# Kernel tuning notes

Measured on AMD Instinct MI355X. Metric: run time of the kernel, lower is better.

## Reference

```python
import jax, jax.numpy as jnp
import numpy as np
from jax import lax

B, S, H, E, P, K, R = 64, 512, 768, 32, 16, 9, 6
HEADS, C1, C2 = 4, 128, 64
FEAT = 4 * C2 + 1  # e1, e2, e1*e2, context (64 each) + log-distance


def _ln(x, g, b):
    m = x.mean(-1, keepdims=True)
    v = ((x - m) ** 2).mean(-1, keepdims=True)
    return (x - m) * lax.rsqrt(v + 1e-5) * g + b


def _gat(x, adj, W, a_s, a_d, bias, heads, cout, concat):
    # Dense GATConv over a small fully-masked entity graph. adj[b,i,j]=edge j->i (incl. self-loops).
    h = jnp.einsum('bef,fhc->behc', x, W.reshape(x.shape[-1], heads, cout))
    s = jnp.einsum('behc,hc->bhe', h, a_s)  # source-node attention term
    d = jnp.einsum('behc,hc->bhe', h, a_d)  # target-node attention term
    logits = jax.nn.leaky_relu(d[:, :, :, None] + s[:, :, None, :], 0.2)  # [b,h,i,j]
    logits = jnp.where(adj[:, None, :, :], logits, -1e9)
    att = jax.nn.softmax(logits, axis=-1)
    out = jnp.einsum('bhij,bjhc->bihc', att, h)
    out = out.reshape(out.shape[0], out.shape[1], heads * cout) if concat else out.mean(2)
    return out + bias


def _crf_nll(em, tags, mask, start, end, trans):
    # torchcrf: loss = -mean log-likelihood. em [B,S,K]; tags [B,S]; mask [B,S] bool.
    emt = jnp.transpose(em, (1, 0, 2))
    tgt = tags.T
    mkt = mask.T.astype(em.dtype)
    num0 = start[tgt[0]] + jnp.take_along_axis(emt[0], tgt[0][:, None], 1)[:, 0]

    def nstep(c, inp):
        ptag, sc = c
        e, t, m = inp
        step = trans[ptag, t] + jnp.take_along_axis(e, t[:, None], 1)[:, 0]
        return (jnp.where(m > 0, t, ptag), sc + step * m), None

    (ltag, num), _ = lax.scan(nstep, (tgt[0], num0), (emt[1:], tgt[1:], mkt[1:]))
    num = num + end[ltag]
    a0 = start[None, :] + emt[0]

    def dstep(a, inp):
        e, m = inp
        nxt = jax.scipy.special.logsumexp(a[:, :, None] + trans[None] + e[:, None, :], axis=1)
        return jnp.where(m[:, None] > 0, nxt, a), None

    aT, _ = lax.scan(dstep, a0, (emt[1:], mkt[1:]))
    Z = jax.scipy.special.logsumexp(aT + end[None], axis=1)
    return jnp.mean(Z - num)


def setup_inputs() -> dict:
    key = jax.random.key(0)
    ks = jax.random.split(key, 24)
    n = lambda i, shape, s=0.05: jax.random.normal(ks[i], shape, jnp.float32) * s
    return {
        'sequence_output': jax.random.normal(ks[0], (B, S, H), jnp.float32),
        'attention_mask': jnp.ones((B, S), jnp.int32),
        'ner_labels': jax.random.randint(ks[1], (B, S), 0, K),
        'entity_start': jax.random.randint(ks[2], (B, E), 0, S - 8),
        'entity_len': jax.random.randint(ks[3], (B, E), 0, 8),
        'pair_e1': jax.random.randint(ks[4], (B, P), 0, E),
        'pair_e2': jax.random.randint(ks[5], (B, P), 0, E),
        'pair_labels': jax.random.randint(ks[6], (B, P), 0, 2),
        'adj_mask': jnp.ones((B, E, E), bool),
        'w_ner1': n(7, (H, 256)), 'b_ner1': jnp.zeros((256,), jnp.float32),
        'w_ner2': n(8, (256, K)), 'b_ner2': jnp.zeros((K,), jnp.float32),
        'crf_start': n(9, (K,), 0.1), 'crf_end': n(10, (K,), 0.1), 'crf_trans': n(11, (K, K), 0.1),
        'w_gat1': n(12, (H, HEADS * C1)), 'a_src1': n(13, (HEADS, C1)), 'a_dst1': n(14, (HEADS, C1)),
        'b_gat1': jnp.zeros((HEADS * C1,), jnp.float32),
        'w_gat2': n(15, (HEADS * C1, C2)), 'a_src2': n(16, (1, C2)), 'a_dst2': n(17, (1, C2)),
        'b_gat2': jnp.zeros((C2,), jnp.float32),
        'w_fe': n(18, (FEAT, 512)), 'b_fe': jnp.zeros((512,), jnp.float32),
        'g_fe': jnp.ones((512,), jnp.float32), 'be_fe': jnp.zeros((512,), jnp.float32),
        'w_rc1': n(19, (R, 512, 256)), 'b_rc1': jnp.zeros((R, 256), jnp.float32),
        'g_rc': jnp.ones((R, 256), jnp.float32), 'be_rc': jnp.zeros((R, 256), jnp.float32),
        'w_rc2': n(20, (R, 256, 1)), 'b_rc2': jnp.zeros((R,), jnp.float32),
    }


def reference(sequence_output, attention_mask, ner_labels, entity_start, entity_len,
              pair_e1, pair_e2, pair_labels, adj_mask,
              w_ner1, b_ner1, w_ner2, b_ner2, crf_start, crf_end, crf_trans,
              w_gat1, a_src1, a_dst1, b_gat1, w_gat2, a_src2, a_dst2, b_gat2,
              w_fe, b_fe, g_fe, be_fe, w_rc1, b_rc1, g_rc, be_rc, w_rc2, b_rc2):
    # NER head (dropout off / eval)
    ner_logits = jnp.maximum(sequence_output @ w_ner1 + b_ner1, 0.0) @ w_ner2 + b_ner2
    ner_loss = _crf_nll(ner_logits, ner_labels, attention_mask.astype(bool),
                        crf_start, crf_end, crf_trans)
    # entity span mean-pool via inclusive cumsum trick
    cs = jnp.concatenate([jnp.zeros((B, 1, H), sequence_output.dtype),
                          jnp.cumsum(sequence_output, axis=1)], axis=1)
    e_end = jnp.clip(entity_start + entity_len, 0, S - 1)
    seg = (jnp.take_along_axis(cs, (e_end + 1)[:, :, None], 1)
           - jnp.take_along_axis(cs, entity_start[:, :, None], 1))
    ent = seg / (e_end - entity_start + 1).astype(sequence_output.dtype)[:, :, None]  # [B,E,H]
    x = _gat(ent, adj_mask, w_gat1, a_src1, a_dst1, b_gat1, HEADS, C1, True)
    x = jnp.maximum(x, 0.0)
    x = _gat(x, adj_mask, w_gat2, a_src2, a_dst2, b_gat2, 1, C2, False)  # [B,E,64]
    x1 = jnp.take_along_axis(x, pair_e1[:, :, None], 1)
    x2 = jnp.take_along_axis(x, pair_e2[:, :, None], 1)
    ctx = jnp.broadcast_to(x.mean(1, keepdims=True), (B, P, C2))
    dist = jnp.log(jnp.abs(pair_e1 - pair_e2).astype(x.dtype) + 1.0)[:, :, None]
    pf = jnp.concatenate([x1, x2, x1 * x2, ctx, dist], axis=-1)  # [B,P,257]
    fe = jax.nn.leaky_relu(_ln(pf @ w_fe + b_fe, g_fe, be_fe), 0.01)
    h1 = jnp.einsum('bpf,rfo->rbpo', fe, w_rc1) + b_rc1[:, None, None, :]
    h1 = jax.nn.leaky_relu(_ln(h1, g_rc[:, None, None, :], be_rc[:, None, None, :]), 0.01)
    z = jnp.einsum('rbpo,ro->rbp', h1, w_rc2[:, :, 0]) + b_rc2[:, None, None]
    y = pair_labels.astype(z.dtype)[None]
    # BCEWithLogitsLoss(pos_weight=2.0), mean per relation type, summed over types
    bce = -(2.0 * y * jax.nn.log_sigmoid(z) + (1.0 - y) * jax.nn.log_sigmoid(-z))
    rel_loss = bce.mean(axis=(1, 2)).sum()
    total = ner_loss + rel_loss
    return ner_logits, z, total
```

## Files before the change

kernel.cpp:

```cpp
#include <hip/hip_runtime.h>
#include <math.h>


#define NB 64
#define NS 512
#define NH 768
#define NE 32
#define NP 16
#define NK 9
#define NR 6
#define NHEADS 4
#define NC1 128
#define NC2 64
#define SEGS 16
#define SEGLEN 32

#define ZOFF 294912
#define TOTOFF 301056

#define WS_ENT   0u
#define WS_WG1T  1572864u
#define WS_X1    2621440u
#define WS_X2    3801088u
#define WS_PF    3956736u
#define WS_FE    4222976u
#define WS_CRF   4747264u
#define WS_REL   4747328u
#define WS_W1T   4747392u
#define WS_WRT   0u
#define WS_WFET  393216u
#define WS_SEG   475136u

typedef __attribute__((ext_vector_type(8))) short bf16x8;
typedef __attribute__((ext_vector_type(4))) float f32x4;

__device__ __forceinline__ unsigned short f2bf(float x) {
  union { float f; unsigned u; } v; v.f = x;
  unsigned r = v.u + 0x7FFFu + ((v.u >> 16) & 1u);
  return (unsigned short)(r >> 16);
}

__device__ __forceinline__ float logsigf(float x) {
  if (x >= 0.f) return -log1pf(__expf(-x));
  return x - log1pf(__expf(x));
}

__global__ __launch_bounds__(256) void k_wt(const float* __restrict__ w1,
    const float* __restrict__ wg1, unsigned short* __restrict__ w1t,
    unsigned short* __restrict__ wg1t) {
  __shared__ unsigned short tr[32 * 776];
  const int t = threadIdx.x;
  const float* src;
  unsigned short* dst;
  int c0, ncol;
  if (blockIdx.x < 8) { src = w1; dst = w1t; ncol = 256; c0 = blockIdx.x * 32; }
  else { src = wg1; dst = wg1t; ncol = 512; c0 = (blockIdx.x - 8) * 32; }
#pragma unroll
  for (int p = 0; p < 24; p++) {
    const int k = p * 32 + (t >> 3), c4 = t & 7;
    const float4 f = *reinterpret_cast<const float4*>(&src[(size_t)k * ncol + c0 + c4 * 4]);
    tr[(c4 * 4 + 0) * 776 + k] = f2bf(f.x);
    tr[(c4 * 4 + 1) * 776 + k] = f2bf(f.y);
    tr[(c4 * 4 + 2) * 776 + k] = f2bf(f.z);
    tr[(c4 * 4 + 3) * 776 + k] = f2bf(f.w);
  }
  __syncthreads();
  const int c = t >> 3, q = t & 7;
#pragma unroll
  for (int i = 0; i < 12; i++) {
    *reinterpret_cast<uint4*>(&dst[(size_t)(c0 + c) * NH + q * 96 + i * 8]) =
        *reinterpret_cast<const uint4*>(&tr[c * 776 + q * 96 + i * 8]);
  }
}

__global__ __launch_bounds__(256) void k_wconv(const float* __restrict__ wrc,
    const float* __restrict__ wfe, unsigned short* __restrict__ wrt,
    unsigned short* __restrict__ wfet) {
  __shared__ unsigned short tr[256 * 72];
  const int t = threadIdx.x;
  if (blockIdx.x < 48) {
    const int r = blockIdx.x >> 3, kt = blockIdx.x & 7;
    const int k0 = kt * 64;
#pragma unroll
    for (int i = 0; i < 16; i++) {
      const int slot = t + 256 * i;
      const int row = slot >> 6, c4 = slot & 63;
      const float4 f = *reinterpret_cast<const float4*>(
          &wrc[((size_t)(r * 512) + k0 + row) * 256 + c4 * 4]);
      tr[(c4 * 4 + 0) * 72 + row] = f2bf(f.x);
      tr[(c4 * 4 + 1) * 72 + row] = f2bf(f.y);
      tr[(c4 * 4 + 2) * 72 + row] = f2bf(f.z);
      tr[(c4 * 4 + 3) * 72 + row] = f2bf(f.w);
    }
    __syncthreads();
#pragma unroll
    for (int i = 0; i < 8; i++) {
      const int slot = t + 256 * i;
      const int col = slot >> 3, q = slot & 7;
      *reinterpret_cast<uint4*>(&wrt[((size_t)(r * 256 + col)) * 512 + k0 + q * 8]) =
          *reinterpret_cast<const uint4*>(&tr[col * 72 + q * 8]);
    }
  } else {
    const int bid = blockIdx.x - 48;
    const int kt = bid % 5, cb = bid / 5;
    const int k0 = kt * 64, c0 = cb * 256;
#pragma unroll
    for (int i = 0; i < 16; i++) {
      const int slot = t + 256 * i;
      const int row = slot >> 6, c4 = slot & 63;
      const int k = k0 + row;
      float4 f = {0.f, 0.f, 0.f, 0.f};
      if (k < 257)
        f = *reinterpret_cast<const float4*>(&wfe[(size_t)k * 512 + c0 + c4 * 4]);
      tr[(c4 * 4 + 0) * 72 + row] = f2bf(f.x);
      tr[(c4 * 4 + 1) * 72 + row] = f2bf(f.y);
      tr[(c4 * 4 + 2) * 72 + row] = f2bf(f.z);
      tr[(c4 * 4 + 3) * 72 + row] = f2bf(f.w);
    }
    __syncthreads();
#pragma unroll
    for (int i = 0; i < 8; i++) {
      const int slot = t + 256 * i;
      const int col = slot >> 3, q = slot & 7;
      *reinterpret_cast<uint4*>(&wfet[((size_t)(c0 + col)) * 320 + k0 + q * 8]) =
          *reinterpret_cast<const uint4*>(&tr[col * 72 + q * 8]);
    }
  }
}

__global__ __launch_bounds__(256) void k_ner(const float* __restrict__ seq,
    const unsigned short* __restrict__ w1t, const float* __restrict__ b1,
    const float* __restrict__ w2, const float* __restrict__ b2,
    float* __restrict__ out) {
  __shared__ unsigned short AsS[64 * 40];
  __shared__ unsigned short BsS[256 * 40];
  __shared__ float zs[64 * 4 * 12];
  const int t = threadIdx.x;
  const int tok0 = blockIdx.x * 64;
  const int w = t >> 6, lane = t & 63, quad = lane >> 4, l15 = lane & 15;

  f32x4 acc[4][4];
#pragma unroll
  for (int r = 0; r < 4; r++)
#pragma unroll
    for (int c = 0; c < 4; c++) acc[r][c] = (f32x4){0.f, 0.f, 0.f, 0.f};

  const int tokA = t >> 2, koffA = (t & 3) * 8;
  const float* aptr = seq + (size_t)(tok0 + tokA) * NH + koffA;

  for (int kt = 0; kt < NH; kt += 32) {
    __syncthreads();
    {
      const float4 f0 = *reinterpret_cast<const float4*>(aptr + kt);
      const float4 f1 = *reinterpret_cast<const float4*>(aptr + kt + 4);
      bf16x8 av;
      av[0] = (short)f2bf(f0.x); av[1] = (short)f2bf(f0.y);
      av[2] = (short)f2bf(f0.z); av[3] = (short)f2bf(f0.w);
      av[4] = (short)f2bf(f1.x); av[5] = (short)f2bf(f1.y);
      av[6] = (short)f2bf(f1.z); av[7] = (short)f2bf(f1.w);
      *reinterpret_cast<bf16x8*>(&AsS[tokA * 40 + koffA]) = av;
    }
#pragma unroll
    for (int i = 0; i < 4; i++) {
      const int q = t + 256 * i;
      const int col = q >> 2, koff = (q & 3) * 8;
      *reinterpret_cast<uint4*>(&BsS[col * 40 + koff]) =
          *reinterpret_cast<const uint4*>(&w1t[(size_t)col * NH + kt + koff]);
    }
    __syncthreads();
    bf16x8 a[4], b[4];
#pragma unroll
    for (int r = 0; r < 4; r++)
      a[r] = *reinterpret_cast<const bf16x8*>(&AsS[(r * 16 + l15) * 40 + quad * 8]);
#pragma unroll
    for (int c = 0; c < 4; c++)
      b[c] = *reinterpret_cast<const bf16x8*>(&BsS[(w * 64 + c * 16 + l15) * 40 + quad * 8]);
#pragma unroll
    for (int r = 0; r < 4; r++)
#pragma unroll
      for (int c = 0; c < 4; c++)
        acc[r][c] = __builtin_amdgcn_mfma_f32_16x16x32_bf16(a[r], b[c], acc[r][c], 0, 0, 0);
  }

  float b1v[4], w2v[4][NK];
#pragma unroll
  for (int c = 0; c < 4; c++) {
    const int col = w * 64 + c * 16 + l15;
    b1v[c] = b1[col];
#pragma unroll
    for (int cc = 0; cc < NK; cc++) w2v[c][cc] = w2[col * NK + cc];
  }
#pragma unroll
  for (int r = 0; r < 4; r++) {
#pragma unroll
    for (int reg = 0; reg < 4; reg++) {
      float p[NK];
#pragma unroll
      for (int cc = 0; cc < NK; cc++) p[cc] = 0.f;
#pragma unroll
      for (int c = 0; c < 4; c++) {
        const float h = fmaxf(acc[r][c][reg] + b1v[c], 0.f);
#pragma unroll
        for (int cc = 0; cc < NK; cc++) p[cc] = fmaf(h, w2v[c][cc], p[cc]);
      }
#pragma unroll
      for (int o = 1; o < 16; o <<= 1)
#pragma unroll
        for (int cc = 0; cc < NK; cc++) p[cc] += __shfl_xor(p[cc], o);
      if (l15 == 0) {
        const int tokr = r * 16 + quad * 4 + reg;
#pragma unroll
        for (int cc = 0; cc < NK; cc++) zs[(tokr * 4 + w) * 12 + cc] = p[cc];
      }
    }
  }
  __syncthreads();
  if (t < 64) {
#pragma unroll
    for (int cc = 0; cc < NK; cc++) {
      const float z = zs[(t * 4 + 0) * 12 + cc] + zs[(t * 4 + 1) * 12 + cc] +
                      zs[(t * 4 + 2) * 12 + cc] + zs[(t * 4 + 3) * 12 + cc] + b2[cc];
      out[(size_t)(tok0 + t) * NK + cc] = z;
    }
  }
}

__global__ __launch_bounds__(128) void k_crf_seg(const float* __restrict__ em,
    const int* __restrict__ mask, const float* __restrict__ trans,
    float* __restrict__ segm) {
  __shared__ float bufA[16 * 81];
  __shared__ float bufB[8 * 81];
  __shared__ float ems[SEGLEN * 9];
  __shared__ int mks[SEGLEN];
  __shared__ float trs[81];
  const int blk = blockIdx.x;
  const int b = blk >> 4, seg = blk & 15;
  const int t = threadIdx.x;
  const int s0 = 1 + seg * SEGLEN;
  const float* emb = em + (size_t)b * NS * NK;
  const int* mk = mask + b * NS;
  if (t < 81) trs[t] = trans[t];
  for (int i = t; i < SEGLEN * 9; i += 128) {
    const int g = s0 * 9 + i;
    ems[i] = (g < NS * 9) ? emb[g] : 0.f;
  }
  if (t < SEGLEN) {
    const int s = s0 + t;
    mks[t] = (s < NS) ? mk[s] : 0;
  }
  __syncthreads();
  for (int idx = t; idx < 16 * 81; idx += 128) {
    const int p = idx / 81, e = idx % 81, i = e / 9, j = e % 9;
    const int la = 2 * p, lb = la + 1;
    const bool ma = mks[la] > 0, mb = mks[lb] > 0;
    float r;
    if (ma && mb) {
      float v[9], mx = -1e30f;
#pragma unroll
      for (int m = 0; m < 9; m++) {
        v[m] = trs[i * 9 + m] + ems[la * 9 + m] + trs[m * 9 + j];
        mx = fmaxf(mx, v[m]);
      }
      float sum = 0.f;
#pragma unroll
      for (int m = 0; m < 9; m++) sum += __expf(v[m] - mx);
      r = mx + __logf(sum) + ems[lb * 9 + j];
    } else if (ma) {
      r = trs[e] + ems[la * 9 + j];
    } else if (mb) {
      r = trs[e] + ems[lb * 9 + j];
    } else {
      r = (i == j) ? 0.f : -1e30f;
    }
    bufA[p * 81 + e] = r;
  }
  float* src = bufA;
  float* dst = bufB;
  for (int n = 16; n > 1; n >>= 1) {
    __syncthreads();
    const int half = n >> 1;
    for (int idx = t; idx < half * 81; idx += 128) {
      const int q = idx / 81, e = idx % 81, i = e / 9, j = e % 9;
      const float* A = src + (size_t)(2 * q) * 81;
      const float* Bm = src + (size_t)(2 * q + 1) * 81;
      float v[9], mx = -1e30f;
#pragma unroll
      for (int m = 0; m < 9; m++) {
        v[m] = A[i * 9 + m] + Bm[m * 9 + j];
        mx = fmaxf(mx, v[m]);
      }
      float sum = 0.f;
#pragma unroll
      for (int m = 0; m < 9; m++) sum += __expf(v[m] - mx);
      dst[q * 81 + e] = mx + __logf(sum);
    }
    float* tmp = src; src = dst; dst = tmp;
  }
  __syncthreads();
  if (t < 81) segm[((size_t)b * SEGS + seg) * 81 + t] = src[t];
}

__global__ __launch_bounds__(64) void k_crf_fin(const float* __restrict__ em,
    const int* __restrict__ tags, const int* __restrict__ mask,
    const float* __restrict__ startv, const float* __restrict__ endv,
    const float* __restrict__ trans, const float* __restrict__ segm,
    float* __restrict__ lossb) {
  __shared__ float sm[SEGS * 81];
  __shared__ float av[16];
  __shared__ float red[2];
  const int b = blockIdx.x, t = threadIdx.x;
  const float* emb = em + (size_t)b * NS * NK;
  const int* mk = mask + b * NS;
  const int* tg = tags + b * NS;
  for (int i = t; i < SEGS * 81; i += 64) sm[i] = segm[(size_t)b * SEGS * 81 + i];
  {
    float num = 0.f;
    int lastS = 0;
#pragma unroll
    for (int o = 0; o < 8; o++) {
      const int s = t * 8 + o;
      if (s >= 1 && mk[s] > 0) {
        const int cur = tg[s], prv = tg[s - 1];
        num += trans[prv * NK + cur] + emb[s * NK + cur];
        lastS = s;
      }
    }
#pragma unroll
    for (int o = 32; o > 0; o >>= 1) {
      num += __shfl_xor(num, o);
      lastS = max(lastS, __shfl_xor(lastS, o));
    }
    if (t == 0) {
      const int t0 = tg[0];
      red[0] = startv[t0] + emb[t0] + num + endv[tg[lastS]];
    }
  }
  __syncthreads();
  if (t < 9) av[t] = startv[t] + emb[t];
  __syncthreads();
  for (int h = 0; h < SEGS; h++) {
    float nv = 0.f;
    if (t < 9) {
      float v[9], mx = -1e30f;
#pragma unroll
      for (int i2 = 0; i2 < 9; i2++) {
        v[i2] = av[i2] + sm[h * 81 + i2 * 9 + t];
        mx = fmaxf(mx, v[i2]);
      }
      float sum = 0.f;
#pragma unroll
      for (int i2 = 0; i2 < 9; i2++) sum += __expf(v[i2] - mx);
      nv = mx + __logf(sum);
    }
    __syncthreads();
    if (t < 9) av[t] = nv;
    __syncthreads();
  }
  if (t == 0) {
    float mx = -1e30f;
#pragma unroll
    for (int j = 0; j < 9; j++) mx = fmaxf(mx, av[j] + endv[j]);
    float sum = 0.f;
#pragma unroll
    for (int j = 0; j < 9; j++) sum += __expf(av[j] + endv[j] - mx);
    lossb[b] = (mx + __logf(sum)) - red[0];
  }
}

__global__ __launch_bounds__(256) void k_ent(const float* __restrict__ seq,
    const int* __restrict__ est, const int* __restrict__ elen,
    unsigned short* __restrict__ entb) {
  const int be = blockIdx.x;
  const int b = be >> 5, e = be & 31;
  const int st = est[b * NE + e];
  int en = st + elen[b * NE + e];
  en = min(max(en, 0), NS - 1);
  const float inv = 1.f / (float)(en - st + 1);
  for (int c = threadIdx.x; c < NH; c += 256) {
    float s = 0.f;
    for (int r = st; r <= en; r++) s += seq[((size_t)b * NS + r) * NH + c];
    entb[((size_t)b * NE + e) * NH + c] = f2bf(s * inv);
  }
}

__global__ __launch_bounds__(256) void k_g1f(const unsigned short* __restrict__ entb,
    const unsigned short* __restrict__ wg1t, const float* __restrict__ as,
    const float* __restrict__ ad, const unsigned char* __restrict__ adj,
    const float* __restrict__ bias, float* __restrict__ x1) {
  __shared__ unsigned short As[32 * 40];
  __shared__ unsigned short Bs[128 * 40];
  __shared__ float Hs[32 * 132];
  __shared__ float Att[32 * 32];
  __shared__ float Sv[32], Dv[32];
  const int b = blockIdx.x >> 2, hd = blockIdx.x & 3;
  const int t = threadIdx.x;
  const int w = t >> 6, lane = t & 63, quad = lane >> 4, l15 = lane & 15;

  f32x4 acc[2][2];
#pragma unroll
  for (int r = 0; r < 2; r++)
#pragma unroll
    for (int c = 0; c < 2; c++) acc[r][c] = (f32x4){0.f, 0.f, 0.f, 0.f};

  const int rowA = t >> 2, koffA = (t & 3) * 8;
  const unsigned short* aptr = entb + ((size_t)(b * NE) + rowA) * NH + koffA;

  for (int kt = 0; kt < NH; kt += 32) {
    __syncthreads();
    if (t < 128) {
      *reinterpret_cast<uint4*>(&As[rowA * 40 + koffA]) =
          *reinterpret_cast<const uint4*>(aptr + kt);
    }
#pragma unroll
    for (int i = 0; i < 2; i++) {
      const int q = t + 256 * i;
      const int col = q >> 2, koff = (q & 3) * 8;
      *reinterpret_cast<uint4*>(&Bs[col * 40 + koff]) =
          *reinterpret_cast<const uint4*>(&wg1t[(size_t)(hd * 128 + col) * NH + kt + koff]);
    }
    __syncthreads();
    bf16x8 a[2], bb[2];
#pragma unroll
    for (int r = 0; r < 2; r++)
      a[r] = *reinterpret_cast<const bf16x8*>(&As[(r * 16 + l15) * 40 + quad * 8]);
#pragma unroll
    for (int c = 0; c < 2; c++)
      bb[c] = *reinterpret_cast<const bf16x8*>(&Bs[(w * 32 + c * 16 + l15) * 40 + quad * 8]);
#pragma unroll
    for (int r = 0; r < 2; r++)
#pragma unroll
      for (int c = 0; c < 2; c++)
        acc[r][c] = __builtin_amdgcn_mfma_f32_16x16x32_bf16(a[r], bb[c], acc[r][c], 0, 0, 0);
  }
#pragma unroll
  for (int r = 0; r < 2; r++)
#pragma unroll
    for (int c = 0; c < 2; c++)
#pragma unroll
      for (int reg = 0; reg < 4; reg++)
        Hs[(r * 16 + quad * 4 + reg) * 132 + w * 32 + c * 16 + l15] = acc[r][c][reg];
  __syncthreads();
  {
    const int e = t >> 3, cg = t & 7;
    float sv = 0.f, dv = 0.f;
#pragma unroll
    for (int c = 0; c < 16; c++) {
      const float h = Hs[e * 132 + cg * 16 + c];
      sv += h * as[hd * NC1 + cg * 16 + c];
      dv += h * ad[hd * NC1 + cg * 16 + c];
    }
#pragma unroll
    for (int o = 1; o < 8; o <<= 1) { sv += __shfl_xor(sv, o); dv += __shfl_xor(dv, o); }
    if (cg == 0) { Sv[e] = sv; Dv[e] = dv; }
  }
  __syncthreads();
  if (t < 32) {
    const int i = t;
    const float di = Dv[i];
    float lg[32];
    float m = -1e30f;
#pragma unroll
    for (int j = 0; j < 32; j++) {
      float v = di + Sv[j];
      v = v >= 0.f ? v : 0.2f * v;
      if (!adj[((size_t)b * NE + i) * NE + j]) v = -1e9f;
      lg[j] = v; m = fmaxf(m, v);
    }
    float sum = 0.f;
#pragma unroll
    for (int j = 0; j < 32; j++) { lg[j] = __expf(lg[j] - m); sum += lg[j]; }
    const float inv = 1.f / sum;
#pragma unroll
    for (int j = 0; j < 32; j++) Att[j * 32 + i] = lg[j] * inv;
  }
  __syncthreads();
  {
    const int tc = t & 31, tr = t >> 5;
#pragma unroll
    for (int i = 0; i < 4; i++) {
      const int row = tr * 4 + i;
      float o0 = bias[hd * NC1 + tc * 4 + 0];
      float o1 = bias[hd * NC1 + tc * 4 + 1];
      float o2 = bias[hd * NC1 + tc * 4 + 2];
      float o3 = bias[hd * NC1 + tc * 4 + 3];
#pragma unroll
      for (int j = 0; j < 32; j++) {
        const float a = Att[j * 32 + row];
        o0 = fmaf(a, Hs[j * 132 + tc * 4 + 0], o0);
        o1 = fmaf(a, Hs[j * 132 + tc * 4 + 1], o1);
        o2 = fmaf(a, Hs[j * 132 + tc * 4 + 2], o2);
        o3 = fmaf(a, Hs[j * 132 + tc * 4 + 3], o3);
      }
      float4 v;
      v.x = fmaxf(o0, 0.f); v.y = fmaxf(o1, 0.f);
      v.z = fmaxf(o2, 0.f); v.w = fmaxf(o3, 0.f);
      *reinterpret_cast<float4*>(&x1[((size_t)b * NE + row) * 512 + hd * 128 + tc * 4]) = v;
    }
  }
}

__global__ __launch_bounds__(256) void k_g2f(const float* __restrict__ x1,
    const float* __restrict__ w, const float* __restrict__ as,
    const float* __restrict__ ad, const unsigned char* __restrict__ adj,
    const float* __restrict__ bias, float* __restrict__ x2) {
  __shared__ float As[32 * 36];
  __shared__ float Bs[32 * 64];
  __shared__ float H2[32 * 68];
  __shared__ float Att[32 * 32];
  __shared__ float Sv[32], Dv[32];
  const int b = blockIdx.x;
  const int t = threadIdx.x;
  const int tc = t & 15, tr = t >> 4;
  float acc[2][4];
#pragma unroll
  for (int i = 0; i < 2; i++)
#pragma unroll
    for (int j = 0; j < 4; j++) acc[i][j] = 0.f;
  for (int kt = 0; kt < 512; kt += 32) {
    __syncthreads();
    {
      const int e = t >> 3, k4 = t & 7;
      *reinterpret_cast<float4*>(&As[e * 36 + k4 * 4]) =
          *reinterpret_cast<const float4*>(&x1[((size_t)b * NE + e) * 512 + kt + k4 * 4]);
    }
#pragma unroll
    for (int i = 0; i < 2; i++) {
      const int slot = t + 256 * i;
      const int row = slot >> 4, cg = slot & 15;
      *reinterpret_cast<float4*>(&Bs[row * 64 + cg * 4]) =
          *reinterpret_cast<const float4*>(&w[(size_t)(kt + row) * NC2 + cg * 4]);
    }
    __syncthreads();
#pragma unroll
    for (int kg = 0; kg < 8; kg++) {
      float4 a[2];
#pragma unroll
      for (int i = 0; i < 2; i++)
        a[i] = *reinterpret_cast<const float4*>(&As[(tr * 2 + i) * 36 + kg * 4]);
#pragma unroll
      for (int k2 = 0; k2 < 4; k2++) {
        const float4 bv = *reinterpret_cast<const float4*>(&Bs[(kg * 4 + k2) * 64 + tc * 4]);
#pragma unroll
        for (int i = 0; i < 2; i++) {
          const float av = reinterpret_cast<const float*>(&a[i])[k2];
          acc[i][0] = fmaf(av, bv.x, acc[i][0]);
          acc[i][1] = fmaf(av, bv.y, acc[i][1]);
          acc[i][2] = fmaf(av, bv.z, acc[i][2]);
          acc[i][3] = fmaf(av, bv.w, acc[i][3]);
        }
      }
    }
  }
  const float4 a4s = *reinterpret_cast<const float4*>(&as[tc * 4]);
  const float4 a4d = *reinterpret_cast<const float4*>(&ad[tc * 4]);
#pragma unroll
  for (int i = 0; i < 2; i++) {
    const int e = tr * 2 + i;
    float4 v;
    v.x = acc[i][0]; v.y = acc[i][1]; v.z = acc[i][2]; v.w = acc[i][3];
    *reinterpret_cast<float4*>(&H2[e * 68 + tc * 4]) = v;
    float sv = v.x * a4s.x + v.y * a4s.y + v.z * a4s.z + v.w * a4s.w;
    float dv = v.x * a4d.x + v.y * a4d.y + v.z * a4d.z + v.w * a4d.w;
#pragma unroll
    for (int o = 8; o > 0; o >>= 1) { sv += __shfl_xor(sv, o); dv += __shfl_xor(dv, o); }
    if (tc == 0) { Sv[e] = sv; Dv[e] = dv; }
  }
  __syncthreads();
  if (t < 32) {
    const int i = t;
    const float di = Dv[i];
    float lg[32];
    float m = -1e30f;
#pragma unroll
    for (int j = 0; j < 32; j++) {
      float v = di + Sv[j];
      v = v >= 0.f ? v : 0.2f * v;
      if (!adj[((size_t)b * NE + i) * NE + j]) v = -1e9f;
      lg[j] = v; m = fmaxf(m, v);
    }
    float sum = 0.f;
#pragma unroll
    for (int j = 0; j < 32; j++) { lg[j] = __expf(lg[j] - m); sum += lg[j]; }
    const float inv = 1.f / sum;
#pragma unroll
    for (int j = 0; j < 32; j++) Att[j * 32 + i] = lg[j] * inv;
  }
  __syncthreads();
#pragma unroll
  for (int i = 0; i < 2; i++) {
    const int row = tr * 2 + i;
    float o0 = bias[tc * 4 + 0];
    float o1 = bias[tc * 4 + 1];
    float o2 = bias[tc * 4 + 2];
    float o3 = bias[tc * 4 + 3];
#pragma unroll
    for (int j = 0; j < 32; j++) {
      const float a = Att[j * 32 + row];
      o0 = fmaf(a, H2[j * 68 + tc * 4 + 0], o0);
      o1 = fmaf(a, H2[j * 68 + tc * 4 + 1], o1);
      o2 = fmaf(a, H2[j * 68 + tc * 4 + 2], o2);
      o3 = fmaf(a, H2[j * 68 + tc * 4 + 3], o3);
    }
    float4 v;
    v.x = o0; v.y = o1; v.z = o2; v.w = o3;
    *reinterpret_cast<float4*>(&x2[((size_t)b * NE + row) * NC2 + tc * 4]) = v;
  }
}

__global__ __launch_bounds__(64) void k_pf(const float* __restrict__ x2,
    const int* __restrict__ pe1, const int* __restrict__ pe2,
    float* __restrict__ pf) {
  const int bp = blockIdx.x;
  const int b = bp >> 4, p = bp & 15;
  const int t = threadIdx.x;
  const int e1 = pe1[b * NP + p], e2 = pe2[b * NP + p];
  const float v1 = x2[((size_t)b * NE + e1) * NC2 + t];
  const float v2 = x2[((size_t)b * NE + e2) * NC2 + t];
  float cs = 0.f;
  for (int e = 0; e < NE; e++) cs += x2[((size_t)b * NE + e) * NC2 + t];
  float* row = pf + (size_t)bp * 260;
  row[t] = v1;
  row[64 + t] = v2;
  row[128 + t] = v1 * v2;
  row[192 + t] = cs * (1.f / NE);
  if (t == 0) row[256] = logf(fabsf((float)(e1 - e2)) + 1.f);
  if (t < 3) row[257 + t] = 0.f;
}

__global__ __launch_bounds__(256) void k_fe(const float* __restrict__ pf,
    const unsigned short* __restrict__ wt, const float* __restrict__ bfe,
    const float* __restrict__ g, const float* __restrict__ be,
    unsigned short* __restrict__ feb) {
  __shared__ unsigned short Af[16 * 320];
  __shared__ float Cs[16 * 520];
  const int b = blockIdx.x, t = threadIdx.x;
  const int w = t >> 6, lane = t & 63, quad = lane >> 4, l15 = lane & 15;
  for (int i = t; i < 16 * 320; i += 256) {
    const int p = i / 320, k = i - p * 320;
    Af[i] = (k < 260) ? f2bf(pf[(size_t)(b * NP + p) * 260 + k]) : (unsigned short)0;
  }
  __syncthreads();
  f32x4 acc[8];
#pragma unroll
  for (int c = 0; c < 8; c++) acc[c] = (f32x4){0.f, 0.f, 0.f, 0.f};
#pragma unroll
  for (int kt = 0; kt < 10; kt++) {
    const bf16x8 a = *reinterpret_cast<const bf16x8*>(&Af[l15 * 320 + kt * 32 + quad * 8]);
#pragma unroll
    for (int c = 0; c < 8; c++) {
      const int col = w * 128 + c * 16 + l15;
      const bf16x8 bv = *reinterpret_cast<const bf16x8*>(&wt[(size_t)col * 320 + kt * 32 + quad * 8]);
      acc[c] = __builtin_amdgcn_mfma_f32_16x16x32_bf16(a, bv, acc[c], 0, 0, 0);
    }
  }
#pragma unroll
  for (int c = 0; c < 8; c++)
#pragma unroll
    for (int reg = 0; reg < 4; reg++)
      Cs[(quad * 4 + reg) * 520 + w * 128 + c * 16 + l15] = acc[c][reg];
  __syncthreads();
  float bfev[8], gv[8], bev[8];
#pragma unroll
  for (int ch = 0; ch < 8; ch++) {
    const int col = ch * 64 + lane;
    bfev[ch] = bfe[col]; gv[ch] = g[col]; bev[ch] = be[col];
  }
#pragma unroll
  for (int pp = 0; pp < 4; pp++) {
    const int p = w * 4 + pp;
    float v[8], s = 0.f, sq = 0.f;
#pragma unroll
    for (int ch = 0; ch < 8; ch++) {
      v[ch] = Cs[p * 520 + ch * 64 + lane] + bfev[ch];
      s += v[ch]; sq += v[ch] * v[ch];
    }
#pragma unroll
    for (int o = 32; o > 0; o >>= 1) { s += __shfl_xor(s, o); sq += __shfl_xor(sq, o); }
    const float mean = s * (1.f / 512.f);
    const float var = sq * (1.f / 512.f) - mean * mean;
    const float rr = rsqrtf(var + 1e-5f);
#pragma unroll
    for (int ch = 0; ch < 8; ch++) {
      float n = (v[ch] - mean) * rr * gv[ch] + bev[ch];
      n = n >= 0.f ? n : 0.01f * n;
      feb[(size_t)(b * NP + p) * 512 + ch * 64 + lane] = f2bf(n);
    }
  }
}

__global__ __launch_bounds__(256) void k_rc(const unsigned short* __restrict__ feb,
    const unsigned short* __restrict__ wrt, const float* __restrict__ b1,
    const float* __restrict__ g, const float* __restrict__ be,
    const float* __restrict__ w2, const float* __restrict__ b2,
    const int* __restrict__ ylab, float* __restrict__ zout, float* __restrict__ relacc) {
  __shared__ unsigned short Af[16 * 520];
  __shared__ float Cs[16 * 264];
  const int blk = blockIdx.x;
  const int r = blk >> 6, b = blk & 63;
  const int t = threadIdx.x;
  const int w = t >> 6, lane = t & 63, quad = lane >> 4, l15 = lane & 15;
#pragma unroll
  for (int i = 0; i < 4; i++) {
    const int slot = t + 256 * i;
    const int p = slot >> 6, q = slot & 63;
    *reinterpret_cast<uint4*>(&Af[p * 520 + q * 8]) =
        *reinterpret_cast<const uint4*>(&feb[(size_t)(b * NP + p) * 512 + q * 8]);
  }
  __syncthreads();
  f32x4 acc[4];
#pragma unroll
  for (int c = 0; c < 4; c++) acc[c] = (f32x4){0.f, 0.f, 0.f, 0.f};
#pragma unroll
  for (int kt = 0; kt < 16; kt++) {
    const bf16x8 a = *reinterpret_cast<const bf16x8*>(&Af[l15 * 520 + kt * 32 + quad * 8]);
#pragma unroll
    for (int c = 0; c < 4; c++) {
      const int col = w * 64 + c * 16 + l15;
      const bf16x8 bv = *reinterpret_cast<const bf16x8*>(
          &wrt[(size_t)(r * 256 + col) * 512 + kt * 32 + quad * 8]);
      acc[c] = __builtin_amdgcn_mfma_f32_16x16x32_bf16(a, bv, acc[c], 0, 0, 0);
    }
  }
#pragma unroll
  for (int c = 0; c < 4; c++)
#pragma unroll
    for (int reg = 0; reg < 4; reg++)
      Cs[(quad * 4 + reg) * 264 + w * 64 + c * 16 + l15] = acc[c][reg];
  __syncthreads();
  float b1v[4], gv[4], bev[4], w2v[4];
#pragma unroll
  for (int ch = 0; ch < 4; ch++) {
    const int col = r * 256 + ch * 64 + lane;
    b1v[ch] = b1[col]; gv[ch] = g[col]; bev[ch] = be[col]; w2v[ch] = w2[col];
  }
  const float b2v = b2[r];
  float local = 0.f;
#pragma unroll
  for (int pp = 0; pp < 4; pp++) {
    const int p = w * 4 + pp;
    float v[4], s = 0.f, sq = 0.f;
#pragma unroll
    for (int ch = 0; ch < 4; ch++) {
      v[ch] = Cs[p * 264 + ch * 64 + lane] + b1v[ch];
      s += v[ch]; sq += v[ch] * v[ch];
    }
#pragma unroll
    for (int o = 32; o > 0; o >>= 1) { s += __shfl_xor(s, o); sq += __shfl_xor(sq, o); }
    const float mean = s * (1.f / 256.f);
    const float var = sq * (1.f / 256.f) - mean * mean;
    const float rr = rsqrtf(var + 1e-5f);
    float zdot = 0.f;
#pragma unroll
    for (int ch = 0; ch < 4; ch++) {
      float n = (v[ch] - mean) * rr * gv[ch] + bev[ch];
      n = n >= 0.f ? n : 0.01f * n;
      zdot = fmaf(n, w2v[ch], zdot);
    }
#pragma unroll
    for (int o = 32; o > 0; o >>= 1) zdot += __shfl_xor(zdot, o);
    if (lane == 0) {
      const float zp = zdot + b2v;
      zout[(size_t)(r * NB + b) * NP + p] = zp;
      const float y = (float)ylab[b * NP + p];
      local += -(2.f * y * logsigf(zp) + (1.f - y) * logsigf(-zp));
    }
  }
  if (lane == 0) atomicAdd(relacc, local * (1.f / (NB * NP)));
}

__global__ __launch_bounds__(64) void k_fin(const float* __restrict__ lossb,
    const float* __restrict__ rel, float* __restrict__ out) {
  float v = lossb[threadIdx.x];
#pragma unroll
  for (int o = 32; o > 0; o >>= 1) v += __shfl_down(v, o);
  if (threadIdx.x == 0) out[TOTOFF] = v * (1.f / NB) + rel[0];
}

extern "C" void kernel_launch(void* const* d_in, const int* in_sizes, int n_in,
                              void* d_out, int out_size, void* d_ws, size_t ws_size,
                              hipStream_t stream) {
  const float* seq = (const float*)d_in[0];
  const int* amask = (const int*)d_in[1];
  const int* nlab = (const int*)d_in[2];
  const int* est = (const int*)d_in[3];
  const int* elen = (const int*)d_in[4];
  const int* pe1 = (const int*)d_in[5];
  const int* pe2 = (const int*)d_in[6];
  const int* plab = (const int*)d_in[7];
  const unsigned char* adj = (const unsigned char*)d_in[8];
  const float* w_ner1 = (const float*)d_in[9];
  const float* b_ner1 = (const float*)d_in[10];
  const float* w_ner2 = (const float*)d_in[11];
  const float* b_ner2 = (const float*)d_in[12];
  const float* crf_start = (const float*)d_in[13];
  const float* crf_end = (const float*)d_in[14];
  const float* crf_trans = (const float*)d_in[15];
  const float* w_gat1 = (const float*)d_in[16];
  const float* a_src1 = (const float*)d_in[17];
  const float* a_dst1 = (const float*)d_in[18];
  const float* b_gat1 = (const float*)d_in[19];
  const float* w_gat2 = (const float*)d_in[20];
  const float* a_src2 = (const float*)d_in[21];
  const float* a_dst2 = (const float*)d_in[22];
  const float* b_gat2 = (const float*)d_in[23];
  const float* w_fe = (const float*)d_in[24];
  const float* b_fe = (const float*)d_in[25];
  const float* g_fe = (const float*)d_in[26];
  const float* be_fe = (const float*)d_in[27];
  const float* w_rc1 = (const float*)d_in[28];
  const float* b_rc1 = (const float*)d_in[29];
  const float* g_rc = (const float*)d_in[30];
  const float* be_rc = (const float*)d_in[31];
  const float* w_rc2 = (const float*)d_in[32];
  const float* b_rc2 = (const float*)d_in[33];

  float* out = (float*)d_out;
  float* ws = (float*)d_ws;
  float* x1 = ws + WS_X1;
  float* x2 = ws + WS_X2;
  float* pf = ws + WS_PF;
  float* crfb = ws + WS_CRF;
  float* rel = ws + WS_REL;
  unsigned short* entb = (unsigned short*)(ws + WS_ENT);
  unsigned short* wg1t = (unsigned short*)(ws + WS_WG1T);
  unsigned short* w1t = (unsigned short*)(ws + WS_W1T);
  unsigned short* feb = (unsigned short*)(ws + WS_FE);
  unsigned short* wrt = (unsigned short*)(ws + WS_WRT);
  unsigned short* wfet = (unsigned short*)(ws + WS_WFET);
  float* segm = ws + WS_SEG;

  hipMemsetAsync(rel, 0, sizeof(float), stream);

  k_wt<<<24, 256, 0, stream>>>(w_ner1, w_gat1, w1t, wg1t);
  k_ner<<<512, 256, 0, stream>>>(seq, w1t, b_ner1, w_ner2, b_ner2, out);
  k_ent<<<NB * NE, 256, 0, stream>>>(seq, est, elen, entb);
  k_g1f<<<NB * NHEADS, 256, 0, stream>>>(entb, wg1t, a_src1, a_dst1, adj, b_gat1, x1);
  k_wconv<<<58, 256, 0, stream>>>(w_rc1, w_fe, wrt, wfet);
  k_crf_seg<<<NB * SEGS, 128, 0, stream>>>(out, amask, crf_trans, segm);
  k_crf_fin<<<NB, 64, 0, stream>>>(out, nlab, amask, crf_start, crf_end, crf_trans,
                                   segm, crfb);
  k_g2f<<<NB, 256, 0, stream>>>(x1, w_gat2, a_src2, a_dst2, adj, b_gat2, x2);
  k_pf<<<NB * NP, 64, 0, stream>>>(x2, pe1, pe2, pf);
  k_fe<<<NB, 256, 0, stream>>>(pf, wfet, b_fe, g_fe, be_fe, feb);
  k_rc<<<NR * NB, 256, 0, stream>>>(feb, wrt, b_rc1, g_rc, be_rc, w_rc2, b_rc2,
                                    plab, out + ZOFF, rel);
  k_fin<<<1, 64, 0, stream>>>(crfb, rel, out);
}
```

Before: 452.0 us.

## Merge independent stages into combined launches and fuse GAT/pair-feature steps

Collapses the pipeline from eleven launches to seven by packing independent work into shared grids. Weight transposes and entity pooling share one kernel. GAT layer 1 runs beside the NER GEMM, now tiled at 32 tokens per block. Weight conversion runs beside the CRF segment pass, and GAT layer 2 (moved to bf16 MFMA with a pre-transposed weight) runs beside the CRF finalisation. Pair-feature construction is folded into k_fe, and x1 is stored as bf16. The aim is to cut launch overhead, fill the GPU with concurrent independent work and drop intermediate buffers, at the cost of heterogeneous blocks with uneven per-block work and a little extra bf16 rounding.

New measurement: 431.9 us. -4.4%, faster.

```diff
diff --git a/kernel.cpp b/kernel.cpp
--- a/kernel.cpp
+++ b/kernel.cpp
@@ -22,7 +22,7 @@
 #define WS_WG1T  1572864u
 #define WS_X1    2621440u
 #define WS_X2    3801088u
-#define WS_PF    3956736u
+#define WS_WG2T  3956736u
 #define WS_FE    4222976u
 #define WS_CRF   4747264u
 #define WS_REL   4747328u
@@ -45,599 +45,597 @@
   return x - log1pf(__expf(x));
 }
 
-__global__ __launch_bounds__(256) void k_wt(const float* __restrict__ w1,
-    const float* __restrict__ wg1, unsigned short* __restrict__ w1t,
-    unsigned short* __restrict__ wg1t) {
+__global__ __launch_bounds__(256) void k_prep(
+    const float* __restrict__ w1, const float* __restrict__ wg1,
+    const float* __restrict__ wg2, const float* __restrict__ seq,
+    const int* __restrict__ est, const int* __restrict__ elen,
+    unsigned short* __restrict__ w1t, unsigned short* __restrict__ wg1t,
+    unsigned short* __restrict__ wg2t, unsigned short* __restrict__ entb) {
   __shared__ unsigned short tr[32 * 776];
-  const int t = threadIdx.x;
-  const float* src;
-  unsigned short* dst;
-  int c0, ncol;
-  if (blockIdx.x < 8) { src = w1; dst = w1t; ncol = 256; c0 = blockIdx.x * 32; }
-  else { src = wg1; dst = wg1t; ncol = 512; c0 = (blockIdx.x - 8) * 32; }
-#pragma unroll
-  for (int p = 0; p < 24; p++) {
-    const int k = p * 32 + (t >> 3), c4 = t & 7;
-    const float4 f = *reinterpret_cast<const float4*>(&src[(size_t)k * ncol + c0 + c4 * 4]);
-    tr[(c4 * 4 + 0) * 776 + k] = f2bf(f.x);
-    tr[(c4 * 4 + 1) * 776 + k] = f2bf(f.y);
-    tr[(c4 * 4 + 2) * 776 + k] = f2bf(f.z);
-    tr[(c4 * 4 + 3) * 776 + k] = f2bf(f.w);
-  }
-  __syncthreads();
-  const int c = t >> 3, q = t & 7;
-#pragma unroll
-  for (int i = 0; i < 12; i++) {
-    *reinterpret_cast<uint4*>(&dst[(size_t)(c0 + c) * NH + q * 96 + i * 8]) =
-        *reinterpret_cast<const uint4*>(&tr[c * 776 + q * 96 + i * 8]);
-  }
-}
-
-__global__ __launch_bounds__(256) void k_wconv(const float* __restrict__ wrc,
-    const float* __restrict__ wfe, unsigned short* __restrict__ wrt,
-    unsigned short* __restrict__ wfet) {
-  __shared__ unsigned short tr[256 * 72];
-  const int t = threadIdx.x;
-  if (blockIdx.x < 48) {
-    const int r = blockIdx.x >> 3, kt = blockIdx.x & 7;
-    const int k0 = kt * 64;
-#pragma unroll
-    for (int i = 0; i < 16; i++) {
-      const int slot = t + 256 * i;
-      const int row = slot >> 6, c4 = slot & 63;
-      const float4 f = *reinterpret_cast<const float4*>(
-          &wrc[((size_t)(r * 512) + k0 + row) * 256 + c4 * 4]);
-      tr[(c4 * 4 + 0) * 72 + row] = f2bf(f.x);
-      tr[(c4 * 4 + 1) * 72 + row] = f2bf(f.y);
-      tr[(c4 * 4 + 2) * 72 + row] = f2bf(f.z);
-      tr[(c4 * 4 + 3) * 72 + row] = f2bf(f.w);
-    }
-    __syncthreads();
-#pragma unroll
-    for (int i = 0; i < 8; i++) {
-      const int slot = t + 256 * i;
-      const int col = slot >> 3, q = slot & 7;
-      *reinterpret_cast<uint4*>(&wrt[((size_t)(r * 256 + col)) * 512 + k0 + q * 8]) =
-          *reinterpret_cast<const uint4*>(&tr[col * 72 + q * 8]);
+  const int bid = blockIdx.x, t = threadIdx.x;
+  if (bid < 26) {
+    const float* src;
+    unsigned short* dst;
+    int c0, ncol, nkt, kdim;
+    if (bid < 8)       { src = w1;  dst = w1t;  ncol = 256; c0 = bid * 32;        nkt = 24; kdim = 768; }
+    else if (bid < 24) { src = wg1; dst = wg1t; ncol = 512; c0 = (bid - 8) * 32;  nkt = 24; kdim = 768; }
+    else               { src = wg2; dst = wg2t; ncol = 64;  c0 = (bid - 24) * 32; nkt = 16; kdim = 512; }
+    for (int p = 0; p < nkt; p++) {
+      const int k = p * 32 + (t >> 3), c4 = t & 7;
+      const float4 f = *reinterpret_cast<const float4*>(&src[(size_t)k * ncol + c0 + c4 * 4]);
+      tr[(c4 * 4 + 0) * 776 + k] = f2bf(f.x);
+      tr[(c4 * 4 + 1) * 776 + k] = f2bf(f.y);
+      tr[(c4 * 4 + 2) * 776 + k] = f2bf(f.z);
+      tr[(c4 * 4 + 3) * 776 + k] = f2bf(f.w);
+    }
+    __syncthreads();
+    const int c = t >> 3, q = t & 7;
+    const int chunk = kdim >> 3;
+    for (int i = 0; i < (chunk >> 3); i++) {
+      *reinterpret_cast<uint4*>(&dst[(size_t)(c0 + c) * kdim + q * chunk + i * 8]) =
+          *reinterpret_cast<const uint4*>(&tr[c * 776 + q * chunk + i * 8]);
     }
   } else {
-    const int bid = blockIdx.x - 48;
-    const int kt = bid % 5, cb = bid / 5;
-    const int k0 = kt * 64, c0 = cb * 256;
-#pragma unroll
-    for (int i = 0; i < 16; i++) {
-      const int slot = t + 256 * i;
-      const int row = slot >> 6, c4 = slot & 63;
-      const int k = k0 + row;
-      float4 f = {0.f, 0.f, 0.f, 0.f};
-      if (k < 257)
-        f = *reinterpret_cast<const float4*>(&wfe[(size_t)k * 512 + c0 + c4 * 4]);
-      tr[(c4 * 4 + 0) * 72 + row] = f2bf(f.x);
-      tr[(c4 * 4 + 1) * 72 + row] = f2bf(f.y);
-      tr[(c4 * 4 + 2) * 72 + row] = f2bf(f.z);
-      tr[(c4 * 4 + 3) * 72 + row] = f2bf(f.w);
-    }
-    __syncthreads();
-#pragma unroll
-    for (int i = 0; i < 8; i++) {
-      const int slot = t + 256 * i;
-      const int col = slot >> 3, q = slot & 7;
-      *reinterpret_cast<uint4*>(&wfet[((size_t)(c0 + col)) * 320 + k0 + q * 8]) =
-          *reinterpret_cast<const uint4*>(&tr[col * 72 + q * 8]);
-    }
-  }
-}
-
-__global__ __launch_bounds__(256) void k_ner(const float* __restrict__ seq,
-    const unsigned short* __restrict__ w1t, const float* __restrict__ b1,
-    const float* __restrict__ w2, const float* __restrict__ b2,
-    float* __restrict__ out) {
-  __shared__ unsigned short AsS[64 * 40];
-  __shared__ unsigned short BsS[256 * 40];
-  __shared__ float zs[64 * 4 * 12];
-  const int t = threadIdx.x;
-  const int tok0 = blockIdx.x * 64;
+    const int be = bid - 26;
+    const int b = be >> 5, e = be & 31;
+    const int st = est[b * NE + e];
+    int en = st + elen[b * NE + e];
+    en = min(max(en, 0), NS - 1);
+    const float inv = 1.f / (float)(en - st + 1);
+    for (int c = t; c < NH; c += 256) {
+      float s = 0.f;
+      for (int r = st; r <= en; r++) s += seq[((size_t)b * NS + r) * NH + c];
+      entb[((size_t)b * NE + e) * NH + c] = f2bf(s * inv);
+    }
+  }
+}
+
+__global__ __launch_bounds__(256) void k_main(
+    const float* __restrict__ seq, const unsigned short* __restrict__ w1t,
+    const float* __restrict__ b1, const float* __restrict__ w2,
+    const float* __restrict__ b2, float* __restrict__ out,
+    const unsigned short* __restrict__ entb, const unsigned short* __restrict__ wg1t,
+    const float* __restrict__ as1, const float* __restrict__ ad1,
+    const unsigned char* __restrict__ adj, const float* __restrict__ bias1,
+    unsigned short* __restrict__ x1b) {
+  __shared__ __align__(16) char smem[34048];
+  const int bid = blockIdx.x, t = threadIdx.x;
   const int w = t >> 6, lane = t & 63, quad = lane >> 4, l15 = lane & 15;
 
-  f32x4 acc[4][4];
-#pragma unroll
-  for (int r = 0; r < 4; r++)
-#pragma unroll
-    for (int c = 0; c < 4; c++) acc[r][c] = (f32x4){0.f, 0.f, 0.f, 0.f};
-
-  const int tokA = t >> 2, koffA = (t & 3) * 8;
-  const float* aptr = seq + (size_t)(tok0 + tokA) * NH + koffA;
-
-  for (int kt = 0; kt < NH; kt += 32) {
+  if (bid < 256) {
+    unsigned short* As = (unsigned short*)smem;
+    unsigned short* Bs = (unsigned short*)(smem + 2560);
+    float* Hs  = (float*)(smem + 12800);
+    float* Att = (float*)(smem + 29696);
+    float* Sv  = (float*)(smem + 33792);
+    float* Dv  = (float*)(smem + 33920);
+    const int b = bid >> 2, hd = bid & 3;
+
+    f32x4 acc[2][2];
+#pragma unroll
+    for (int r = 0; r < 2; r++)
+#pragma unroll
+      for (int c = 0; c < 2; c++) acc[r][c] = (f32x4){0.f, 0.f, 0.f, 0.f};
+
+    const int rowA = t >> 2, koffA = (t & 3) * 8;
+    const unsigned short* aptr = entb + ((size_t)(b * NE) + rowA) * NH + koffA;
+
+    for (int kt = 0; kt < NH; kt += 32) {
+      __syncthreads();
+      if (t < 128) {
+        *reinterpret_cast<uint4*>(&As[rowA * 40 + koffA]) =
+            *reinterpret_cast<const uint4*>(aptr + kt);
+      }
+#pragma unroll
+      for (int i = 0; i < 2; i++) {
+        const int q = t + 256 * i;
+        const int col = q >> 2, koff = (q & 3) * 8;
+        *reinterpret_cast<uint4*>(&Bs[col * 40 + koff]) =
+            *reinterpret_cast<const uint4*>(&wg1t[(size_t)(hd * 128 + col) * NH + kt + koff]);
+      }
+      __syncthreads();
+      bf16x8 a[2], bb[2];
+#pragma unroll
+      for (int r = 0; r < 2; r++)
+        a[r] = *reinterpret_cast<const bf16x8*>(&As[(r * 16 + l15) * 40 + quad * 8]);
+#pragma unroll
+      for (int c = 0; c < 2; c++)
+        bb[c] = *reinterpret_cast<const bf16x8*>(&Bs[(w * 32 + c * 16 + l15) * 40 + quad * 8]);
+#pragma unroll
+      for (int r = 0; r < 2; r++)
+#pragma unroll
+        for (int c = 0; c < 2; c++)
+          acc[r][c] = __builtin_amdgcn_mfma_f32_16x16x32_bf16(a[r], bb[c], acc[r][c], 0, 0, 0);
+    }
+#pragma unroll
+    for (int r = 0; r < 2; r++)
+#pragma unroll
+      for (int c = 0; c < 2; c++)
+#pragma unroll
+        for (int reg = 0; reg < 4; reg++)
+          Hs[(r * 16 + quad * 4 + reg) * 132 + w * 32 + c * 16 + l15] = acc[r][c][reg];
     __syncthreads();
     {
-      const float4 f0 = *reinterpret_cast<const float4*>(aptr + kt);
-      const float4 f1 = *reinterpret_cast<const float4*>(aptr + kt + 4);
-      bf16x8 av;
-      av[0] = (short)f2bf(f0.x); av[1] = (short)f2bf(f0.y);
-      av[2] = (short)f2bf(f0.z); av[3] = (short)f2bf(f0.w);
-      av[4] = (short)f2bf(f1.x); av[5] = (short)f2bf(f1.y);
-      av[6] = (short)f2bf(f1.z); av[7] = (short)f2bf(f1.w);
-      *reinterpret_cast<bf16x8*>(&AsS[tokA * 40 + koffA]) = av;
-    }
-#pragma unroll
-    for (int i = 0; i < 4; i++) {
-      const int q = t + 256 * i;
-      const int col = q >> 2, koff = (q & 3) * 8;
-      *reinterpret_cast<uint4*>(&BsS[col * 40 + koff]) =
-          *reinterpret_cast<const uint4*>(&w1t[(size_t)col * NH + kt + koff]);
-    }
-    __syncthreads();
-    bf16x8 a[4], b[4];
-#pragma unroll
-    for (int r = 0; r < 4; r++)
-      a[r] = *reinterpret_cast<const bf16x8*>(&AsS[(r * 16 + l15) * 40 + quad * 8]);
-#pragma unroll
-    for (int c = 0; c < 4; c++)
-      b[c] = *reinterpret_cast<const bf16x8*>(&BsS[(w * 64 + c * 16 + l15) * 40 + quad * 8]);
-#pragma unroll
-    for (int r = 0; r < 4; r++)
+      const int e = t >> 3, cg = t & 7;
+      float sv = 0.f, dv = 0.f;
+#pragma unroll
+      for (int c = 0; c < 16; c++) {
+        const float h = Hs[e * 132 + cg * 16 + c];
+        sv += h * as1[hd * NC1 + cg * 16 + c];
+        dv += h * ad1[hd * NC1 + cg * 16 + c];
+      }
+#pragma unroll
+      for (int o = 1; o < 8; o <<= 1) { sv += __shfl_xor(sv, o); dv += __shfl_xor(dv, o); }
+      if (cg == 0) { Sv[e] = sv; Dv[e] = dv; }
+    }
+    __syncthreads();
+    if (t < 32) {
+      const int i = t;
+      const float di = Dv[i];
+      float lg[32];
+      float m = -1e30f;
+#pragma unroll
+      for (int j = 0; j < 32; j++) {
+        float v = di + Sv[j];
+        v = v >= 0.f ? v : 0.2f * v;
+        if (!adj[((size_t)b * NE + i) * NE + j]) v = -1e9f;
+        lg[j] = v; m = fmaxf(m, v);
+      }
+      float sum = 0.f;
+#pragma unroll
+      for (int j = 0; j < 32; j++) { lg[j] = __expf(lg[j] - m); sum += lg[j]; }
+      const float inv = 1.f / sum;
+#pragma unroll
+      for (int j = 0; j < 32; j++) Att[j * 32 + i] = lg[j] * inv;
+    }
+    __syncthreads();
+    {
+      const int tc = t & 31, tr2 = t >> 5;
+#pragma unroll
+      for (int i = 0; i < 4; i++) {
+        const int row = tr2 * 4 + i;
+        float o0 = bias1[hd * NC1 + tc * 4 + 0];
+        float o1 = bias1[hd * NC1 + tc * 4 + 1];
+        float o2 = bias1[hd * NC1 + tc * 4 + 2];
+        float o3 = bias1[hd * NC1 + tc * 4 + 3];
+#pragma unroll
+        for (int j = 0; j < 32; j++) {
+          const float a = Att[j * 32 + row];
+          o0 = fmaf(a, Hs[j * 132 + tc * 4 + 0], o0);
+          o1 = fmaf(a, Hs[j * 132 + tc * 4 + 1], o1);
+          o2 = fmaf(a, Hs[j * 132 + tc * 4 + 2], o2);
+          o3 = fmaf(a, Hs[j * 132 + tc * 4 + 3], o3);
+        }
+        uint2 v;
+        v.x = (unsigned)f2bf(fmaxf(o0, 0.f)) | ((unsigned)f2bf(fmaxf(o1, 0.f)) << 16);
+        v.y = (unsigned)f2bf(fmaxf(o2, 0.f)) | ((unsigned)f2bf(fmaxf(o3, 0.f)) << 16);
+        *reinterpret_cast<uint2*>(&x1b[((size_t)b * NE + row) * 512 + hd * 128 + tc * 4]) = v;
+      }
+    }
+  } else {
+    unsigned short* AsS = (unsigned short*)smem;
+    unsigned short* BsS = (unsigned short*)(smem + 2560);
+    float* zs = (float*)(smem + 23040);
+    const int tok0 = (bid - 256) * 32;
+
+    f32x4 acc[2][4];
+#pragma unroll
+    for (int r = 0; r < 2; r++)
+#pragma unroll
+      for (int c = 0; c < 4; c++) acc[r][c] = (f32x4){0.f, 0.f, 0.f, 0.f};
+
+    const int tokA = t >> 3, koffA = (t & 7) * 4;
+    const float* aptr = seq + (size_t)(tok0 + tokA) * NH + koffA;
+
+    for (int kt = 0; kt < NH; kt += 32) {
+      __syncthreads();
+      {
+        const float4 f0 = *reinterpret_cast<const float4*>(aptr + kt);
+        uint2 v;
+        v.x = (unsigned)f2bf(f0.x) | ((unsigned)f2bf(f0.y) << 16);
+        v.y = (unsigned)f2bf(f0.z) | ((unsigned)f2bf(f0.w) << 16);
+        *reinterpret_cast<uint2*>(&AsS[tokA * 40 + koffA]) = v;
+      }
+#pragma unroll
+      for (int i = 0; i < 4; i++) {
+        const int q = t + 256 * i;
+        const int col = q >> 2, koff = (q & 3) * 8;
+        *reinterpret_cast<uint4*>(&BsS[col * 40 + koff]) =
+            *reinterpret_cast<const uint4*>(&w1t[(size_t)col * NH + kt + koff]);
+      }
+      __syncthreads();
+      bf16x8 a[2], b[4];
+#pragma unroll
+      for (int r = 0; r < 2; r++)
+        a[r] = *reinterpret_cast<const bf16x8*>(&AsS[(r * 16 + l15) * 40 + quad * 8]);
 #pragma unroll
       for (int c = 0; c < 4; c++)
-        acc[r][c] = __builtin_amdgcn_mfma_f32_16x16x32_bf16(a[r], b[c], acc[r][c], 0, 0, 0);
-  }
-
-  float b1v[4], w2v[4][NK];
-#pragma unroll
-  for (int c = 0; c < 4; c++) {
-    const int col = w * 64 + c * 16 + l15;
-    b1v[c] = b1[col];
-#pragma unroll
-    for (int cc = 0; cc < NK; cc++) w2v[c][cc] = w2[col * NK + cc];
-  }
-#pragma unroll
-  for (int r = 0; r < 4; r++) {
-#pragma unroll
-    for (int reg = 0; reg < 4; reg++) {
-      float p[NK];
-#pragma unroll
-      for (int cc = 0; cc < NK; cc++) p[cc] = 0.f;
-#pragma unroll
-      for (int c = 0; c < 4; c++) {
-        const float h = fmaxf(acc[r][c][reg] + b1v[c], 0.f);
-#pragma unroll
-        for (int cc = 0; cc < NK; cc++) p[cc] = fmaf(h, w2v[c][cc], p[cc]);
-      }
-#pragma unroll
-      for (int o = 1; o < 16; o <<= 1)
-#pragma unroll
-        for (int cc = 0; cc < NK; cc++) p[cc] += __shfl_xor(p[cc], o);
-      if (l15 == 0) {
-        const int tokr = r * 16 + quad * 4 + reg;
-#pragma unroll
-        for (int cc = 0; cc < NK; cc++) zs[(tokr * 4 + w) * 12 + cc] = p[cc];
-      }
-    }
-  }
-  __syncthreads();
-  if (t < 64) {
-#pragma unroll
-    for (int cc = 0; cc < NK; cc++) {
-      const float z = zs[(t * 4 + 0) * 12 + cc] + zs[(t * 4 + 1) * 12 + cc] +
-                      zs[(t * 4 + 2) * 12 + cc] + zs[(t * 4 + 3) * 12 + cc] + b2[cc];
-      out[(size_t)(tok0 + t) * NK + cc] = z;
-    }
-  }
-}
-
-__global__ __launch_bounds__(128) void k_crf_seg(const float* __restrict__ em,
-    const int* __restrict__ mask, const float* __restrict__ trans,
-    float* __restrict__ segm) {
-  __shared__ float bufA[16 * 81];
-  __shared__ float bufB[8 * 81];
-  __shared__ float ems[SEGLEN * 9];
-  __shared__ int mks[SEGLEN];
-  __shared__ float trs[81];
-  const int blk = blockIdx.x;
-  const int b = blk >> 4, seg = blk & 15;
-  const int t = threadIdx.x;
-  const int s0 = 1 + seg * SEGLEN;
-  const float* emb = em + (size_t)b * NS * NK;
-  const int* mk = mask + b * NS;
-  if (t < 81) trs[t] = trans[t];
-  for (int i = t; i < SEGLEN * 9; i += 128) {
-    const int g = s0 * 9 + i;
-    ems[i] = (g < NS * 9) ? emb[g] : 0.f;
-  }
-  if (t < SEGLEN) {
-    const int s = s0 + t;
-    mks[t] = (s < NS) ? mk[s] : 0;
-  }
-  __syncthreads();
-  for (int idx = t; idx < 16 * 81; idx += 128) {
-    const int p = idx / 81, e = idx % 81, i = e / 9, j = e % 9;
-    const int la = 2 * p, lb = la + 1;
-    const bool ma = mks[la] > 0, mb = mks[lb] > 0;
-    float r;
-    if (ma && mb) {
-      float v[9], mx = -1e30f;
-#pragma unroll
-      for (int m = 0; m < 9; m++) {
-        v[m] = trs[i * 9 + m] + ems[la * 9 + m] + trs[m * 9 + j];
-        mx = fmaxf(mx, v[m]);
+        b[c] = *reinterpret_cast<const bf16x8*>(&BsS[(w * 64 + c * 16 + l15) * 40 + quad * 8]);
+#pragma unroll
+      for (int r = 0; r < 2; r++)
+#pragma unroll
+        for (int c = 0; c < 4; c++)
+          acc[r][c] = __builtin_amdgcn_mfma_f32_16x16x32_bf16(a[r], b[c], acc[r][c], 0, 0, 0);
+    }
+
+    float b1v[4], w2v[4][NK];
+#pragma unroll
+    for (int c = 0; c < 4; c++) {
+      const int col = w * 64 + c * 16 + l15;
+      b1v[c] = b1[col];
+#pragma unroll
+      for (int cc = 0; cc < NK; cc++) w2v[c][cc] = w2[col * NK + cc];
+    }
+#pragma unroll
+    for (int r = 0; r < 2; r++) {
+#pragma unroll
+      for (int reg = 0; reg < 4; reg++) {
+        float p[NK];
+#pragma unroll
+        for (int cc = 0; cc < NK; cc++) p[cc] = 0.f;
+#pragma unroll
+        for (int c = 0; c < 4; c++) {
+          const float h = fmaxf(acc[r][c][reg] + b1v[c], 0.f);
+#pragma unroll
+          for (int cc = 0; cc < NK; cc++) p[cc] = fmaf(h, w2v[c][cc], p[cc]);
+        }
+#pragma unroll
+        for (int o = 1; o < 16; o <<= 1)
+#pragma unroll
+          for (int cc = 0; cc < NK; cc++) p[cc] += __shfl_xor(p[cc], o);
+        if (l15 == 0) {
+          const int tokr = r * 16 + quad * 4 + reg;
+#pragma unroll
+          for (int cc = 0; cc < NK; cc++) zs[(tokr * 4 + w) * 12 + cc] = p[cc];
+        }
+      }
+    }
+    __syncthreads();
+    if (t < 32) {
+#pragma unroll
+      for (int cc = 0; cc < NK; cc++) {
+        const float z = zs[(t * 4 + 0) * 12 + cc] + zs[(t * 4 + 1) * 12 + cc] +
+                        zs[(t * 4 + 2) * 12 + cc] + zs[(t * 4 + 3) * 12 + cc] + b2[cc];
+        out[(size_t)(tok0 + t) * NK + cc] = z;
+      }
+    }
+  }
+}
+
+__global__ __launch_bounds__(256) void k_mid(
+    const float* __restrict__ wrc, const float* __restrict__ wfe,
+    unsigned short* __restrict__ wrt, unsigned short* __restrict__ wfet,
+    const float* __restrict__ em, const int* __restrict__ mask,
+    const float* __restrict__ trans, float* __restrict__ segm) {
+  __shared__ __align__(16) char smem[36864];
+  const int bid = blockIdx.x, t = threadIdx.x;
+  if (bid < 58) {
+    unsigned short* tr = (unsigned short*)smem;
+    if (bid < 48) {
+      const int r = bid >> 3, kt = bid & 7;
+      const int k0 = kt * 64;
+#pragma unroll
+      for (int i = 0; i < 16; i++) {
+        const int slot = t + 256 * i;
+        const int row = slot >> 6, c4 = slot & 63;
+        const float4 f = *reinterpret_cast<const float4*>(
+            &wrc[((size_t)(r * 512) + k0 + row) * 256 + c4 * 4]);
+        tr[(c4 * 4 + 0) * 72 + row] = f2bf(f.x);
+        tr[(c4 * 4 + 1) * 72 + row] = f2bf(f.y);
+        tr[(c4 * 4 + 2) * 72 + row] = f2bf(f.z);
+        tr[(c4 * 4 + 3) * 72 + row] = f2bf(f.w);
+      }
+      __syncthreads();
+#pragma unroll
+      for (int i = 0; i < 8; i++) {
+        const int slot = t + 256 * i;
+        const int col = slot >> 3, q = slot & 7;
+        *reinterpret_cast<uint4*>(&wrt[((size_t)(r * 256 + col)) * 512 + k0 + q * 8]) =
+            *reinterpret_cast<const uint4*>(&tr[col * 72 + q * 8]);
+      }
+    } else {
+      const int b2 = bid - 48;
+      const int kt = b2 % 5, cb = b2 / 5;
+      const int k0 = kt * 64, c0 = cb * 256;
+#pragma unroll
+      for (int i = 0; i < 16; i++) {
+        const int slot = t + 256 * i;
+        const int row = slot >> 6, c4 = slot & 63;
+        const int k = k0 + row;
+        float4 f = {0.f, 0.f, 0.f, 0.f};
+        if (k < 257)
+          f = *reinterpret_cast<const float4*>(&wfe[(size_t)k * 512 + c0 + c4 * 4]);
+        tr[(c4 * 4 + 0) * 72 + row] = f2bf(f.x);
+        tr[(c4 * 4 + 1) * 72 + row] = f2bf(f.y);
+        tr[(c4 * 4 + 2) * 72 + row] = f2bf(f.z);
+        tr[(c4 * 4 + 3) * 72 + row] = f2bf(f.w);
+      }
+      __syncthreads();
+#pragma unroll
+      for (int i = 0; i < 8; i++) {
+        const int slot = t + 256 * i;
+        const int col = slot >> 3, q = slot & 7;
+        *reinterpret_cast<uint4*>(&wfet[((size_t)(c0 + col)) * 320 + k0 + q * 8]) =
+            *reinterpret_cast<const uint4*>(&tr[col * 72 + q * 8]);
+      }
+    }
+  } else {
+    float* bufA = (float*)smem;
+    float* bufB = (float*)(smem + 5184);
+    float* ems  = (float*)(smem + 7776);
+    int*   mks  = (int*)(smem + 8928);
+    float* trs  = (float*)(smem + 9056);
+    const int blk = bid - 58;
+    const int b = blk >> 4, seg = blk & 15;
+    const int s0 = 1 + seg * SEGLEN;
+    const float* emb = em + (size_t)b * NS * NK;
+    const int* mk = mask + b * NS;
+    if (t < 81) trs[t] = trans[t];
+    for (int i = t; i < SEGLEN * 9; i += 256) {
+      const int g = s0 * 9 + i;
+      ems[i] = (g < NS * 9) ? emb[g] : 0.f;
+    }
+    if (t < SEGLEN) {
+      const int s = s0 + t;
+      mks[t] = (s < NS) ? mk[s] : 0;
+    }
+    __syncthreads();
+    for (int idx = t; idx < 16 * 81; idx += 256) {
+      const int p = idx / 81, e = idx % 81, i = e / 9, j = e % 9;
+      const int la = 2 * p, lb = la + 1;
+      const bool ma = mks[la] > 0, mb = mks[lb] > 0;
+      float r;
+      if (ma && mb) {
+        float v[9], mx = -1e30f;
+#pragma unroll
+        for (int m = 0; m < 9; m++) {
+          v[m] = trs[i * 9 + m] + ems[la * 9 + m] + trs[m * 9 + j];
+          mx = fmaxf(mx, v[m]);
+        }
+        float sum = 0.f;
+#pragma unroll
+        for (int m = 0; m < 9; m++) sum += __expf(v[m] - mx);
+        r = mx + __logf(sum) + ems[lb * 9 + j];
+      } else if (ma) {
+        r = trs[e] + ems[la * 9 + j];
+      } else if (mb) {
+        r = trs[e] + ems[lb * 9 + j];
+      } else {
+        r = (i == j) ? 0.f : -1e30f;
+      }
+      bufA[p * 81 + e] = r;
+    }
+    float* src = bufA;
+    float* dst = bufB;
+    for (int n = 16; n > 1; n >>= 1) {
+      __syncthreads();
+      const int half = n >> 1;
+      for (int idx = t; idx < half * 81; idx += 256) {
+        const int q = idx / 81, e = idx % 81, i = e / 9, j = e % 9;
+        const float* A = src + (size_t)(2 * q) * 81;
+        const float* Bm = src + (size_t)(2 * q + 1) * 81;
+        float v[9], mx = -1e30f;
+#pragma unroll
+        for (int m = 0; m < 9; m++) {
+          v[m] = A[i * 9 + m] + Bm[m * 9 + j];
+          mx = fmaxf(mx, v[m]);
+        }
+        float sum = 0.f;
+#pragma unroll
+        for (int m = 0; m < 9; m++) sum += __expf(v[m] - mx);
+        dst[q * 81 + e] = mx + __logf(sum);
+      }
+      float* tmp = src; src = dst; dst = tmp;
+    }
+    __syncthreads();
+    if (t < 81) segm[((size_t)b * SEGS + seg) * 81 + t] = src[t];
+  }
+}
+
+__global__ __launch_bounds__(256) void k_late(
+    const unsigned short* __restrict__ x1b, const unsigned short* __restrict__ wg2t,
+    const float* __restrict__ as2, const float* __restrict__ ad2,
+    const unsigned char* __restrict__ adj, const float* __restrict__ bias2,
+    float* __restrict__ x2,
+    const float* __restrict__ em, const int* __restrict__ tags,
+    const int* __restrict__ mask, const float* __restrict__ startv,
+    const float* __restrict__ endv, const float* __restrict__ trans,
+    const float* __restrict__ segm, float* __restrict__ lossb) {
+  __shared__ __align__(16) char smem[20736];
+  const int bid = blockIdx.x, t = threadIdx.x;
+  if (bid < 64) {
+    unsigned short* As = (unsigned short*)smem;
+    unsigned short* Bs = (unsigned short*)(smem + 2560);
+    float* H2  = (float*)(smem + 7680);
+    float* Att = (float*)(smem + 16384);
+    float* Sv  = (float*)(smem + 20480);
+    float* Dv  = (float*)(smem + 20608);
+    const int b = bid;
+    const int w = t >> 6, lane = t & 63, quad = lane >> 4, l15 = lane & 15;
+
+    f32x4 acc[2];
+#pragma unroll
+    for (int r = 0; r < 2; r++) acc[r] = (f32x4){0.f, 0.f, 0.f, 0.f};
+
+    const int rowA = t >> 2, koffA = (t & 3) * 8;
+    const unsigned short* aptr = x1b + ((size_t)(b * NE) + rowA) * 512 + koffA;
+
+    for (int kt = 0; kt < 512; kt += 32) {
+      __syncthreads();
+      if (t < 128) {
+        *reinterpret_cast<uint4*>(&As[rowA * 40 + koffA]) =
+            *reinterpret_cast<const uint4*>(aptr + kt);
+      }
+      {
+        const int col = t >> 2, koff = (t & 3) * 8;
+        *reinterpret_cast<uint4*>(&Bs[col * 40 + koff]) =
+            *reinterpret_cast<const uint4*>(&wg2t[(size_t)col * 512 + kt + koff]);
+      }
+      __syncthreads();
+      const bf16x8 a0 = *reinterpret_cast<const bf16x8*>(&As[l15 * 40 + quad * 8]);
+      const bf16x8 a1 = *reinterpret_cast<const bf16x8*>(&As[(16 + l15) * 40 + quad * 8]);
+      const bf16x8 bb = *reinterpret_cast<const bf16x8*>(&Bs[(w * 16 + l15) * 40 + quad * 8]);
+      acc[0] = __builtin_amdgcn_mfma_f32_16x16x32_bf16(a0, bb, acc[0], 0, 0, 0);
+      acc[1] = __builtin_amdgcn_mfma_f32_16x16x32_bf16(a1, bb, acc[1], 0, 0, 0);
+    }
+#pragma unroll
+    for (int r = 0; r < 2; r++)
+#pragma unroll
+      for (int reg = 0; reg < 4; reg++)
+        H2[(r * 16 + quad * 4 + reg) * 68 + w * 16 + l15] = acc[r][reg];
+    __syncthreads();
+    {
+      const int e = t >> 3, cg = t & 7;
+      float sv = 0.f, dv = 0.f;
+#pragma unroll
+      for (int c = 0; c < 8; c++) {
+        const float h = H2[e * 68 + cg * 8 + c];
+        sv += h * as2[cg * 8 + c];
+        dv += h * ad2[cg * 8 + c];
+      }
+#pragma unroll
+      for (int o = 1; o < 8; o <<= 1) { sv += __shfl_xor(sv, o); dv += __shfl_xor(dv, o); }
+      if (cg == 0) { Sv[e] = sv; Dv[e] = dv; }
+    }
+    __syncthreads();
+    if (t < 32) {
+      const int i = t;
+      const float di = Dv[i];
+      float lg[32];
+      float m = -1e30f;
+#pragma unroll
+      for (int j = 0; j < 32; j++) {
+        float v = di + Sv[j];
+        v = v >= 0.f ? v : 0.2f * v;
+        if (!adj[((size_t)b * NE + i) * NE + j]) v = -1e9f;
+        lg[j] = v; m = fmaxf(m, v);
       }
       float sum = 0.f;
 #pragma unroll
-      for (int m = 0; m < 9; m++) sum += __expf(v[m] - mx);
-      r = mx + __logf(sum) + ems[lb * 9 + j];
-    } else if (ma) {
-      r = trs[e] + ems[la * 9 + j];
-    } else if (mb) {
-      r = trs[e] + ems[lb * 9 + j];
-    } else {
-      r = (i == j) ? 0.f : -1e30f;
-    }
-    bufA[p * 81 + e] = r;
-  }
-  float* src = bufA;
-  float* dst = bufB;
-  for (int n = 16; n > 1; n >>= 1) {
-    __syncthreads();
-    const int half = n >> 1;
-    for (int idx = t; idx < half * 81; idx += 128) {
-      const int q = idx / 81, e = idx % 81, i = e / 9, j = e % 9;
-      const float* A = src + (size_t)(2 * q) * 81;
-      const float* Bm = src + (size_t)(2 * q + 1) * 81;
-      float v[9], mx = -1e30f;
-#pragma unroll
-      for (int m = 0; m < 9; m++) {
-        v[m] = A[i * 9 + m] + Bm[m * 9 + j];
-        mx = fmaxf(mx, v[m]);
-      }
+      for (int j = 0; j < 32; j++) { lg[j] = __expf(lg[j] - m); sum += lg[j]; }
+      const float inv = 1.f / sum;
+#pragma unroll
+      for (int j = 0; j < 32; j++) Att[j * 32 + i] = lg[j] * inv;
+    }
+    __syncthreads();
+    {
+      const int tc = t & 15, tr2 = t >> 4;
+#pragma unroll
+      for (int i = 0; i < 2; i++) {
+        const int row = tr2 * 2 + i;
+        float o0 = bias2[tc * 4 + 0];
+        float o1 = bias2[tc * 4 + 1];
+        float o2 = bias2[tc * 4 + 2];
+        float o3 = bias2[tc * 4 + 3];
+#pragma unroll
+        for (int j = 0; j < 32; j++) {
+          const float a = Att[j * 32 + row];
+          o0 = fmaf(a, H2[j * 68 + tc * 4 + 0], o0);
+          o1 = fmaf(a, H2[j * 68 + tc * 4 + 1], o1);
+          o2 = fmaf(a, H2[j * 68 + tc * 4 + 2], o2);
+          o3 = fmaf(a, H2[j * 68 + tc * 4 + 3], o3);
+        }
+        float4 v;
+        v.x = o0; v.y = o1; v.z = o2; v.w = o3;
+        *reinterpret_cast<float4*>(&x2[((size_t)b * NE + row) * NC2 + tc * 4]) = v;
+      }
+    }
+  } else {
+    float* sm  = (float*)smem;
+    float* av  = (float*)(smem + 5184);
+    float* red = (float*)(smem + 5248);
+    const int b = bid - 64;
+    const float* emb = em + (size_t)b * NS * NK;
+    const int* mk = mask + b * NS;
+    const int* tg = tags + b * NS;
+    for (int i = t; i < SEGS * 81; i += 256) sm[i] = segm[(size_t)b * SEGS * 81 + i];
+    if (t < 64) {
+      float num = 0.f;
+      int lastS = 0;
+#pragma unroll
+      for (int o = 0; o < 8; o++) {
+        const int s = t * 8 + o;
+        if (s >= 1 && mk[s] > 0) {
+          const int cur = tg[s], prv = tg[s - 1];
+          num += trans[prv * NK + cur] + emb[s * NK + cur];
+          lastS = s;
+        }
+      }
+#pragma unroll
+      for (int o = 32; o > 0; o >>= 1) {
+        num += __shfl_xor(num, o);
+        lastS = max(lastS, __shfl_xor(lastS, o));
+      }
+      if (t == 0) {
+        const int t0 = tg[0];
+        red[0] = startv[t0] + emb[t0] + num + endv[tg[lastS]];
+      }
+    }
+    __syncthreads();
+    if (t < 9) av[t] = startv[t] + emb[t];
+    __syncthreads();
+    for (int h = 0; h < SEGS; h++) {
+      float nv = 0.f;
+      if (t < 9) {
+        float v[9], mx = -1e30f;
+#pragma unroll
+        for (int i2 = 0; i2 < 9; i2++) {
+          v[i2] = av[i2] + sm[h * 81 + i2 * 9 + t];
+          mx = fmaxf(mx, v[i2]);
+        }
+        float sum = 0.f;
+#pragma unroll
+        for (int i2 = 0; i2 < 9; i2++) sum += __expf(v[i2] - mx);
+        nv = mx + __logf(sum);
+      }
+      __syncthreads();
+      if (t < 9) av[t] = nv;
+      __syncthreads();
+    }
+    if (t == 0) {
+      float mx = -1e30f;
+#pragma unroll
+      for (int j = 0; j < 9; j++) mx = fmaxf(mx, av[j] + endv[j]);
       float sum = 0.f;
 #pragma unroll
-      for (int m = 0; m < 9; m++) sum += __expf(v[m] - mx);
-      dst[q * 81 + e] = mx + __logf(sum);
-    }
-    float* tmp = src; src = dst; dst = tmp;
-  }
-  __syncthreads();
-  if (t < 81) segm[((size_t)b * SEGS + seg) * 81 + t] = src[t];
-}
-
-__global__ __launch_bounds__(64) void k_crf_fin(const float* __restrict__ em,
-    const int* __restrict__ tags, const int* __restrict__ mask,
-    const float* __restrict__ startv, const float* __restrict__ endv,
-    const float* __restrict__ trans, const float* __restrict__ segm,
-    float* __restrict__ lossb) {
-  __shared__ float sm[SEGS * 81];
-  __shared__ float av[16];
-  __shared__ float red[2];
-  const int b = blockIdx.x, t = threadIdx.x;
-  const float* emb = em + (size_t)b * NS * NK;
-  const int* mk = mask + b * NS;
-  const int* tg = tags + b * NS;
-  for (int i = t; i < SEGS * 81; i += 64) sm[i] = segm[(size_t)b * SEGS * 81 + i];
-  {
-    float num = 0.f;
-    int lastS = 0;
-#pragma unroll
-    for (int o = 0; o < 8; o++) {
-      const int s = t * 8 + o;
-      if (s >= 1 && mk[s] > 0) {
-        const int cur = tg[s], prv = tg[s - 1];
-        num += trans[prv * NK + cur] + emb[s * NK + cur];
-        lastS = s;
-      }
-    }
-#pragma unroll
-    for (int o = 32; o > 0; o >>= 1) {
-      num += __shfl_xor(num, o);
-      lastS = max(lastS, __shfl_xor(lastS, o));
-    }
-    if (t == 0) {
-      const int t0 = tg[0];
-      red[0] = startv[t0] + emb[t0] + num + endv[tg[lastS]];
-    }
-  }
-  __syncthreads();
-  if (t < 9) av[t] = startv[t] + emb[t];
-  __syncthreads();
-  for (int h = 0; h < SEGS; h++) {
-    float nv = 0.f;
-    if (t < 9) {
-      float v[9], mx = -1e30f;
-#pragma unroll
-      for (int i2 = 0; i2 < 9; i2++) {
-        v[i2] = av[i2] + sm[h * 81 + i2 * 9 + t];
-        mx = fmaxf(mx, v[i2]);
-      }
-      float sum = 0.f;
-#pragma unroll
-      for (int i2 = 0; i2 < 9; i2++) sum += __expf(v[i2] - mx);
-      nv = mx + __logf(sum);
-    }
-    __syncthreads();
-    if (t < 9) av[t] = nv;
-    __syncthreads();
-  }
-  if (t == 0) {
-    float mx = -1e30f;
-#pragma unroll
-    for (int j = 0; j < 9; j++) mx = fmaxf(mx, av[j] + endv[j]);
-    float sum = 0.f;
-#pragma unroll
-    for (int j = 0; j < 9; j++) sum += __expf(av[j] + endv[j] - mx);
-    lossb[b] = (mx + __logf(sum)) - red[0];
-  }
-}
-
-__global__ __launch_bounds__(256) void k_ent(const float* __restrict__ seq,
-    const int* __restrict__ est, const int* __restrict__ elen,
-    unsigned short* __restrict__ entb) {
-  const int be = blockIdx.x;
-  const int b = be >> 5, e = be & 31;
-  const int st = est[b * NE + e];
-  int en = st + elen[b * NE + e];
-  en = min(max(en, 0), NS - 1);
-  const float inv = 1.f / (float)(en - st + 1);
-  for (int c = threadIdx.x; c < NH; c += 256) {
-    float s = 0.f;
-    for (int r = st; r <= en; r++) s += seq[((size_t)b * NS + r) * NH + c];
-    entb[((size_t)b * NE + e) * NH + c] = f2bf(s * inv);
-  }
-}
-
-__global__ __launch_bounds__(256) void k_g1f(const unsigned short* __restrict__ entb,
-    const unsigned short* __restrict__ wg1t, const float* __restrict__ as,
-    const float* __restrict__ ad, const unsigned char* __restrict__ adj,
-    const float* __restrict__ bias, float* __restrict__ x1) {
-  __shared__ unsigned short As[32 * 40];
-  __shared__ unsigned short Bs[128 * 40];
-  __shared__ float Hs[32 * 132];
-  __shared__ float Att[32 * 32];
-  __shared__ float Sv[32], Dv[32];
-  const int b = blockIdx.x >> 2, hd = blockIdx.x & 3;
-  const int t = threadIdx.x;
-  const int w = t >> 6, lane = t & 63, quad = lane >> 4, l15 = lane & 15;
-
-  f32x4 acc[2][2];
-#pragma unroll
-  for (int r = 0; r < 2; r++)
-#pragma unroll
-    for (int c = 0; c < 2; c++) acc[r][c] = (f32x4){0.f, 0.f, 0.f, 0.f};
-
-  const int rowA = t >> 2, koffA = (t & 3) * 8;
-  const unsigned short* aptr = entb + ((size_t)(b * NE) + rowA) * NH + koffA;
-
-  for (int kt = 0; kt < NH; kt += 32) {
-    __syncthreads();
-    if (t < 128) {
-      *reinterpret_cast<uint4*>(&As[rowA * 40 + koffA]) =
-          *reinterpret_cast<const uint4*>(aptr + kt);
-    }
-#pragma unroll
-    for (int i = 0; i < 2; i++) {
-      const int q = t + 256 * i;
-      const int col = q >> 2, koff = (q & 3) * 8;
-      *reinterpret_cast<uint4*>(&Bs[col * 40 + koff]) =
-          *reinterpret_cast<const uint4*>(&wg1t[(size_t)(hd * 128 + col) * NH + kt + koff]);
-    }
-    __syncthreads();
-    bf16x8 a[2], bb[2];
-#pragma unroll
-    for (int r = 0; r < 2; r++)
-      a[r] = *reinterpret_cast<const bf16x8*>(&As[(r * 16 + l15) * 40 + quad * 8]);
-#pragma unroll
-    for (int c = 0; c < 2; c++)
-      bb[c] = *reinterpret_cast<const bf16x8*>(&Bs[(w * 32 + c * 16 + l15) * 40 + quad * 8]);
-#pragma unroll
-    for (int r = 0; r < 2; r++)
-#pragma unroll
-      for (int c = 0; c < 2; c++)
-        acc[r][c] = __builtin_amdgcn_mfma_f32_16x16x32_bf16(a[r], bb[c], acc[r][c], 0, 0, 0);
-  }
-#pragma unroll
-  for (int r = 0; r < 2; r++)
-#pragma unroll
-    for (int c = 0; c < 2; c++)
-#pragma unroll
-      for (int reg = 0; reg < 4; reg++)
-        Hs[(r * 16 + quad * 4 + reg) * 132 + w * 32 + c * 16 + l15] = acc[r][c][reg];
-  __syncthreads();
-  {
-    const int e = t >> 3, cg = t & 7;
-    float sv = 0.f, dv = 0.f;
-#pragma unroll
-    for (int c = 0; c < 16; c++) {
-      const float h = Hs[e * 132 + cg * 16 + c];
-      sv += h * as[hd * NC1 + cg * 16 + c];
-      dv += h * ad[hd * NC1 + cg * 16 + c];
-    }
-#pragma unroll
-    for (int o = 1; o < 8; o <<= 1) { sv += __shfl_xor(sv, o); dv += __shfl_xor(dv, o); }
-    if (cg == 0) { Sv[e] = sv; Dv[e] = dv; }
-  }
-  __syncthreads();
-  if (t < 32) {
-    const int i = t;
-    const float di = Dv[i];
-    float lg[32];
-    float m = -1e30f;
-#pragma unroll
-    for (int j = 0; j < 32; j++) {
-      float v = di + Sv[j];
-      v = v >= 0.f ? v : 0.2f * v;
-      if (!adj[((size_t)b * NE + i) * NE + j]) v = -1e9f;
-      lg[j] = v; m = fmaxf(m, v);
-    }
-    float sum = 0.f;
-#pragma unroll
-    for (int j = 0; j < 32; j++) { lg[j] = __expf(lg[j] - m); sum += lg[j]; }
-    const float inv = 1.f / sum;
-#pragma unroll
-    for (int j = 0; j < 32; j++) Att[j * 32 + i] = lg[j] * inv;
-  }
-  __syncthreads();
-  {
-    const int tc = t & 31, tr = t >> 5;
-#pragma unroll
-    for (int i = 0; i < 4; i++) {
-      const int row = tr * 4 + i;
-      float o0 = bias[hd * NC1 + tc * 4 + 0];
-      float o1 = bias[hd * NC1 + tc * 4 + 1];
-      float o2 = bias[hd * NC1 + tc * 4 + 2];
-      float o3 = bias[hd * NC1 + tc * 4 + 3];
-#pragma unroll
-      for (int j = 0; j < 32; j++) {
-        const float a = Att[j * 32 + row];
-        o0 = fmaf(a, Hs[j * 132 + tc * 4 + 0], o0);
-        o1 = fmaf(a, Hs[j * 132 + tc * 4 + 1], o1);
-        o2 = fmaf(a, Hs[j * 132 + tc * 4 + 2], o2);
-        o3 = fmaf(a, Hs[j * 132 + tc * 4 + 3], o3);
-      }
-      float4 v;
-      v.x = fmaxf(o0, 0.f); v.y = fmaxf(o1, 0.f);
-      v.z = fmaxf(o2, 0.f); v.w = fmaxf(o3, 0.f);
-      *reinterpret_cast<float4*>(&x1[((size_t)b * NE + row) * 512 + hd * 128 + tc * 4]) = v;
-    }
-  }
-}
-
-__global__ __launch_bounds__(256) void k_g2f(const float* __restrict__ x1,
-    const float* __restrict__ w, const float* __restrict__ as,
-    const float* __restrict__ ad, const unsigned char* __restrict__ adj,
-    const float* __restrict__ bias, float* __restrict__ x2) {
-  __shared__ float As[32 * 36];
-  __shared__ float Bs[32 * 64];
-  __shared__ float H2[32 * 68];
-  __shared__ float Att[32 * 32];
-  __shared__ float Sv[32], Dv[32];
-  const int b = blockIdx.x;
-  const int t = threadIdx.x;
-  const int tc = t & 15, tr = t >> 4;
-  float acc[2][4];
-#pragma unroll
-  for (int i = 0; i < 2; i++)
-#pragma unroll
-    for (int j = 0; j < 4; j++) acc[i][j] = 0.f;
-  for (int kt = 0; kt < 512; kt += 32) {
-    __syncthreads();
-    {
-      const int e = t >> 3, k4 = t & 7;
-      *reinterpret_cast<float4*>(&As[e * 36 + k4 * 4]) =
-          *reinterpret_cast<const float4*>(&x1[((size_t)b * NE + e) * 512 + kt + k4 * 4]);
-    }
-#pragma unroll
-    for (int i = 0; i < 2; i++) {
-      const int slot = t + 256 * i;
-      const int row = slot >> 4, cg = slot & 15;
-      *reinterpret_cast<float4*>(&Bs[row * 64 + cg * 4]) =
-          *reinterpret_cast<const float4*>(&w[(size_t)(kt + row) * NC2 + cg * 4]);
-    }
-    __syncthreads();
-#pragma unroll
-    for (int kg = 0; kg < 8; kg++) {
-      float4 a[2];
-#pragma unroll
-      for (int i = 0; i < 2; i++)
-        a[i] = *reinterpret_cast<const float4*>(&As[(tr * 2 + i) * 36 + kg * 4]);
-#pragma unroll
-      for (int k2 = 0; k2 < 4; k2++) {
-        const float4 bv = *reinterpret_cast<const float4*>(&Bs[(kg * 4 + k2) * 64 + tc * 4]);
-#pragma unroll
-        for (int i = 0; i < 2; i++) {
-          const float av = reinterpret_cast<const float*>(&a[i])[k2];
-          acc[i][0] = fmaf(av, bv.x, acc[i][0]);
-          acc[i][1] = fmaf(av, bv.y, acc[i][1]);
-          acc[i][2] = fmaf(av, bv.z, acc[i][2]);
-          acc[i][3] = fmaf(av, bv.w, acc[i][3]);
-        }
-      }
-    }
-  }
-  const float4 a4s = *reinterpret_cast<const float4*>(&as[tc * 4]);
-  const float4 a4d = *reinterpret_cast<const float4*>(&ad[tc * 4]);
-#pragma unroll
-  for (int i = 0; i < 2; i++) {
-    const int e = tr * 2 + i;
-    float4 v;
-    v.x = acc[i][0]; v.y = acc[i][1]; v.z = acc[i][2]; v.w = acc[i][3];
-    *reinterpret_cast<float4*>(&H2[e * 68 + tc * 4]) = v;
-    float sv = v.x * a4s.x + v.y * a4s.y + v.z * a4s.z + v.w * a4s.w;
-    float dv = v.x * a4d.x + v.y * a4d.y + v.z * a4d.z + v.w * a4d.w;
-#pragma unroll
-    for (int o = 8; o > 0; o >>= 1) { sv += __shfl_xor(sv, o); dv += __shfl_xor(dv, o); }
-    if (tc == 0) { Sv[e] = sv; Dv[e] = dv; }
-  }
-  __syncthreads();
-  if (t < 32) {
-    const int i = t;
-    const float di = Dv[i];
-    float lg[32];
-    float m = -1e30f;
-#pragma unroll
-    for (int j = 0; j < 32; j++) {
-      float v = di + Sv[j];
-      v = v >= 0.f ? v : 0.2f * v;
-      if (!adj[((size_t)b * NE + i) * NE + j]) v = -1e9f;
-      lg[j] = v; m = fmaxf(m, v);
-    }
-    float sum = 0.f;
-#pragma unroll
-    for (int j = 0; j < 32; j++) { lg[j] = __expf(lg[j] - m); sum += lg[j]; }
-    const float inv = 1.f / sum;
-#pragma unroll
-    for (int j = 0; j < 32; j++) Att[j * 32 + i] = lg[j] * inv;
-  }
-  __syncthreads();
-#pragma unroll
-  for (int i = 0; i < 2; i++) {
-    const int row = tr * 2 + i;
-    float o0 = bias[tc * 4 + 0];
-    float o1 = bias[tc * 4 + 1];
-    float o2 = bias[tc * 4 + 2];
-    float o3 = bias[tc * 4 + 3];
-#pragma unroll
-    for (int j = 0; j < 32; j++) {
-      const float a = Att[j * 32 + row];
-      o0 = fmaf(a, H2[j * 68 + tc * 4 + 0], o0);
-      o1 = fmaf(a, H2[j * 68 + tc * 4 + 1], o1);
-      o2 = fmaf(a, H2[j * 68 + tc * 4 + 2], o2);
-      o3 = fmaf(a, H2[j * 68 + tc * 4 + 3], o3);
-    }
-    float4 v;
-    v.x = o0; v.y = o1; v.z = o2; v.w = o3;
-    *reinterpret_cast<float4*>(&x2[((size_t)b * NE + row) * NC2 + tc * 4]) = v;
-  }
-}
-
-__global__ __launch_bounds__(64) void k_pf(const float* __restrict__ x2,
+      for (int j = 0; j < 9; j++) sum += __expf(av[j] + endv[j] - mx);
+      lossb[b] = (mx + __logf(sum)) - red[0];
+    }
+  }
+}
+
+__global__ __launch_bounds__(256) void k_fe(const float* __restrict__ x2,
     const int* __restrict__ pe1, const int* __restrict__ pe2,
-    float* __restrict__ pf) {
-  const int bp = blockIdx.x;
-  const int b = bp >> 4, p = bp & 15;
-  const int t = threadIdx.x;
-  const int e1 = pe1[b * NP + p], e2 = pe2[b * NP + p];
-  const float v1 = x2[((size_t)b * NE + e1) * NC2 + t];
-  const float v2 = x2[((size_t)b * NE + e2) * NC2 + t];
-  float cs = 0.f;
-  for (int e = 0; e < NE; e++) cs += x2[((size_t)b * NE + e) * NC2 + t];
-  float* row = pf + (size_t)bp * 260;
-  row[t] = v1;
-  row[64 + t] = v2;
-  row[128 + t] = v1 * v2;
-  row[192 + t] = cs * (1.f / NE);
-  if (t == 0) row[256] = logf(fabsf((float)(e1 - e2)) + 1.f);
-  if (t < 3) row[257 + t] = 0.f;
-}
-
-__global__ __launch_bounds__(256) void k_fe(const float* __restrict__ pf,
     const unsigned short* __restrict__ wt, const float* __restrict__ bfe,
     const float* __restrict__ g, const float* __restrict__ be,
     unsigned short* __restrict__ feb) {
   __shared__ unsigned short Af[16 * 320];
   __shared__ float Cs[16 * 520];
+  __shared__ float ctxs[64];
   const int b = blockIdx.x, t = threadIdx.x;
   const int w = t >> 6, lane = t & 63, quad = lane >> 4, l15 = lane & 15;
+  if (t < 64) {
+    float cs = 0.f;
+    for (int e = 0; e < NE; e++) cs += x2[((size_t)b * NE + e) * NC2 + t];
+    ctxs[t] = cs * (1.f / NE);
+  }
+  __syncthreads();
   for (int i = t; i < 16 * 320; i += 256) {
     const int p = i / 320, k = i - p * 320;
-    Af[i] = (k < 260) ? f2bf(pf[(size_t)(b * NP + p) * 260 + k]) : (unsigned short)0;
+    unsigned short o = 0;
+    if (k < 260) {
+      const int e1 = pe1[b * NP + p], e2 = pe2[b * NP + p];
+      float v;
+      if (k < 64) v = x2[((size_t)b * NE + e1) * NC2 + k];
+      else if (k < 128) v = x2[((size_t)b * NE + e2) * NC2 + (k - 64)];
+      else if (k < 192) v = x2[((size_t)b * NE + e1) * NC2 + (k - 128)] *
+                            x2[((size_t)b * NE + e2) * NC2 + (k - 128)];
+      else if (k < 256) v = ctxs[k - 192];
+      else if (k == 256) v = logf(fabsf((float)(e1 - e2)) + 1.f);
+      else v = 0.f;
+      o = f2bf(v);
+    }
+    Af[i] = o;
   }
   __syncthreads();
   f32x4 acc[8];
@@ -816,13 +814,13 @@
 
   float* out = (float*)d_out;
   float* ws = (float*)d_ws;
-  float* x1 = ws + WS_X1;
   float* x2 = ws + WS_X2;
-  float* pf = ws + WS_PF;
   float* crfb = ws + WS_CRF;
   float* rel = ws + WS_REL;
   unsigned short* entb = (unsigned short*)(ws + WS_ENT);
   unsigned short* wg1t = (unsigned short*)(ws + WS_WG1T);
+  unsigned short* wg2t = (unsigned short*)(ws + WS_WG2T);
+  unsigned short* x1b = (unsigned short*)(ws + WS_X1);
   unsigned short* w1t = (unsigned short*)(ws + WS_W1T);
   unsigned short* feb = (unsigned short*)(ws + WS_FE);
   unsigned short* wrt = (unsigned short*)(ws + WS_WRT);
@@ -831,17 +829,15 @@
 
   hipMemsetAsync(rel, 0, sizeof(float), stream);
 
-  k_wt<<<24, 256, 0, stream>>>(w_ner1, w_gat1, w1t, wg1t);
-  k_ner<<<512, 256, 0, stream>>>(seq, w1t, b_ner1, w_ner2, b_ner2, out);
-  k_ent<<<NB * NE, 256, 0, stream>>>(seq, est, elen, entb);
-  k_g1f<<<NB * NHEADS, 256, 0, stream>>>(entb, wg1t, a_src1, a_dst1, adj, b_gat1, x1);
-  k_wconv<<<58, 256, 0, stream>>>(w_rc1, w_fe, wrt, wfet);
-  k_crf_seg<<<NB * SEGS, 128, 0, stream>>>(out, amask, crf_trans, segm);
-  k_crf_fin<<<NB, 64, 0, stream>>>(out, nlab, amask, crf_start, crf_end, crf_trans,
-                                   segm, crfb);
-  k_g2f<<<NB, 256, 0, stream>>>(x1, w_gat2, a_src2, a_dst2, adj, b_gat2, x2);
-  k_pf<<<NB * NP, 64, 0, stream>>>(x2, pe1, pe2, pf);
-  k_fe<<<NB, 256, 0, stream>>>(pf, wfet, b_fe, g_fe, be_fe, feb);
+  k_prep<<<2074, 256, 0, stream>>>(w_ner1, w_gat1, w_gat2, seq, est, elen,
+                                   w1t, wg1t, wg2t, entb);
+  k_main<<<1280, 256, 0, stream>>>(seq, w1t, b_ner1, w_ner2, b_ner2, out,
+                                   entb, wg1t, a_src1, a_dst1, adj, b_gat1, x1b);
+  k_mid<<<1082, 256, 0, stream>>>(w_rc1, w_fe, wrt, wfet, out, amask, crf_trans, segm);
+  k_late<<<128, 256, 0, stream>>>(x1b, wg2t, a_src2, a_dst2, adj, b_gat2, x2,
+                                  out, nlab, amask, crf_start, crf_end, crf_trans,
+                                  segm, crfb);
+  k_fe<<<64, 256, 0, stream>>>(x2, pe1, pe2, wfet, b_fe, g_fe, be_fe, feb);
   k_rc<<<NR * NB, 256, 0, stream>>>(feb, wrt, b_rc1, g_rc, be_rc, w_rc2, b_rc2,
                                     plab, out + ZOFF, rel);
   k_fin<<<1, 64, 0, stream>>>(crfb, rel, out);
```
